# Kernel optimization log

Measured on AMD Instinct MI355X. Metric: run time of the kernel, lower is better.

The kernel has to match this reference:

```python
import jax, jax.numpy as jnp
import numpy as np

FEAT = 128
N_RBF = 20
CUTOFF = 5.0
NUM_CONV = 3
N_ATOMS = 8000
N_EDGES = 160000
N_MOLS = 100
EPS = 1e-15


def silu(x):
    return x * jax.nn.sigmoid(x)


def setup_inputs() -> dict:
    key = jax.random.key(0)
    ks = jax.random.split(key, 16)
    F = FEAT

    def w(k, shape, fan_in):
        return jax.random.normal(k, shape, dtype=jnp.float32) / np.sqrt(fan_in).astype(np.float32)

    nbr0 = jax.random.randint(ks[12], (N_EDGES,), 0, N_ATOMS)
    # avoid self-edges (would give zero distance)
    nbr1 = (nbr0 + 1 + jax.random.randint(ks[13], (N_EDGES,), 0, N_ATOMS - 1)) % N_ATOMS
    return {
        "xyz": jax.random.uniform(ks[0], (N_ATOMS, 3), dtype=jnp.float32) * 10.0,
        "emb_table": jax.random.normal(ks[1], (100, F), dtype=jnp.float32),
        "msg_w1": w(ks[2], (NUM_CONV, F, F), F),
        "msg_b1": jnp.zeros((NUM_CONV, F), jnp.float32),
        "msg_w2": w(ks[3], (NUM_CONV, F, 3 * F), F),
        "msg_b2": jnp.zeros((NUM_CONV, 3 * F), jnp.float32),
        "rbf_w": w(ks[4], (NUM_CONV, N_RBF, 3 * F), N_RBF),
        "rbf_b": jnp.zeros((NUM_CONV, 3 * F), jnp.float32),
        "upd_u": w(ks[5], (NUM_CONV, F, F), F),
        "upd_v": w(ks[6], (NUM_CONV, F, F), F),
        "upd_w1": w(ks[7], (NUM_CONV, 2 * F, F), 2 * F),
        "upd_b1": jnp.zeros((NUM_CONV, F), jnp.float32),
        "upd_w2": w(ks[8], (NUM_CONV, F, 3 * F), F),
        "upd_b2": jnp.zeros((NUM_CONV, 3 * F), jnp.float32),
        "ro_w1": w(ks[9], (F, F // 2), F),
        "ro_b1": jnp.zeros((F // 2,), jnp.float32),
        "ro_w2": w(ks[10], (F // 2, 1), F // 2),
        "ro_b2": jnp.zeros((1,), jnp.float32),
        "z": jax.random.randint(ks[11], (N_ATOMS,), 0, 100),
        "nbrs": jnp.stack([nbr0, nbr1], axis=1),
        "mol_idx": jnp.sort(jax.random.randint(ks[14], (N_ATOMS,), 0, N_MOLS)),
    }


def painn_forward(xyz, emb_table, msg_w1, msg_b1, msg_w2, msg_b2, rbf_w, rbf_b,
                  upd_u, upd_v, upd_w1, upd_b1, upd_w2, upd_b2,
                  ro_w1, ro_b1, ro_w2, ro_b2, z, nbrs, mol_idx):
    F = FEAT
    N = xyz.shape[0]
    # r_ij points from nbrs[:,0] (center i) to nbrs[:,1] (neighbor j)
    r_ij = xyz[nbrs[:, 1]] - xyz[nbrs[:, 0]]            # (E, 3)
    d = jnp.sqrt(jnp.sum(r_ij * r_ij, axis=-1))         # (E,)
    unit = r_ij / d[:, None]                            # (E, 3)
    # PaiNN sinc radial basis: sin(n*pi*d/cutoff)/d, n = 1..n_rbf
    n = jnp.arange(1, N_RBF + 1, dtype=jnp.float32)
    rbf = jnp.sin(n[None, :] * jnp.pi * d[:, None] / CUTOFF) / d[:, None]  # (E, n_rbf)
    # cosine cutoff envelope
    env = jnp.where(d <= CUTOFF, 0.5 * (jnp.cos(jnp.pi * d / CUTOFF) + 1.0), 0.0)

    s = emb_table[z]                                    # (N, F)
    v = jnp.zeros((N, F, 3), dtype=s.dtype)             # (N, F, 3)

    for i in range(NUM_CONV):
        # ---- message block ----
        phi = silu(s @ msg_w1[i] + msg_b1[i]) @ msg_w2[i] + msg_b2[i]   # (N, 3F)
        w_s = (rbf @ rbf_w[i] + rbf_b[i]) * env[:, None]                # (E, 3F)
        inv = (phi[nbrs[:, 1]] * w_s).reshape(-1, 3, F)                 # (E, 3, F)
        split0 = inv[:, 0, :][..., None]                                # (E, F, 1)
        split1 = inv[:, 1, :]                                           # (E, F)
        split2 = inv[:, 2, :][..., None]                                # (E, F, 1)
        dv_ij = split2 * unit[:, None, :] + split0 * v[nbrs[:, 1]]      # (E, F, 3)
        ds = jax.ops.segment_sum(split1, nbrs[:, 0], num_segments=N)
        dv = jax.ops.segment_sum(dv_ij, nbrs[:, 0], num_segments=N)
        s = s + ds
        v = v + dv
        # ---- update block ----
        u_v = jnp.einsum('nfd,fg->ngd', v, upd_u[i])                    # (N, F, 3)
        v_v = jnp.einsum('nfd,fg->ngd', v, upd_v[i])                    # (N, F, 3)
        v_v_norm = jnp.sqrt(jnp.sum(v_v * v_v, axis=-1) + EPS)          # (N, F)
        stack = jnp.concatenate([s, v_v_norm], axis=-1)                 # (N, 2F)
        a = (silu(stack @ upd_w1[i] + upd_b1[i]) @ upd_w2[i] + upd_b2[i]).reshape(-1, 3, F)
        a_vv = a[:, 0, :][..., None]
        a_sv = a[:, 1, :]
        a_ss = a[:, 2, :]
        dv_u = u_v * a_vv
        ds_u = jnp.sum(u_v * v_v, axis=-1) * a_sv + a_ss
        s = s + ds_u
        v = v + dv_u

    # readout MLP + per-molecule sum pool (SumPool)
    atom_e = silu(s @ ro_w1 + ro_b1) @ ro_w2 + ro_b2                    # (N, 1)
    energy = jax.ops.segment_sum(atom_e, mol_idx, num_segments=N_MOLS)  # (N_MOLS, 1)
    return energy


def reference(xyz, emb_table, msg_w1, msg_b1, msg_w2, msg_b2, rbf_w, rbf_b,
              upd_u, upd_v, upd_w1, upd_b1, upd_w2, upd_b2,
              ro_w1, ro_b1, ro_w2, ro_b2, z, nbrs, mol_idx):
    return painn_forward(xyz, emb_table, msg_w1, msg_b1, msg_w2, msg_b2, rbf_w, rbf_b,
                         upd_u, upd_v, upd_w1, upd_b1, upd_w2, upd_b2,
                         ro_w1, ro_b1, ro_w2, ro_b2, z, nbrs, mol_idx)
```

## Files before the change

### kernel.cpp

```cpp
#include <hip/hip_runtime.h>

static constexpr int F = 128;
static constexpr int N_RBF = 20;
static constexpr int N_ATOMS = 8000;
static constexpr int NP = 8064;
static constexpr int N_EDGES = 160000;
static constexpr int N_MOLS = 100;
static constexpr float CUTOFF = 5.0f;
static constexpr size_t NFC = (size_t)NP * F;
static constexpr int REC = 28;
#define PIF 3.14159265358979323846f

typedef __attribute__((ext_vector_type(8))) short bf16x8;
typedef __attribute__((ext_vector_type(4))) float f32x4;
typedef unsigned short ushort_t;
typedef unsigned int uint_t;

__device__ __forceinline__ float silu_f(float x) { return x / (1.f + __expf(-x)); }

__device__ __forceinline__ ushort_t f2bf(float x) {
    union { float f; uint_t u; } v; v.f = x;
    uint_t r = v.u + 0x7fffu + ((v.u >> 16) & 1u);
    return (ushort_t)(r >> 16);
}
__device__ __forceinline__ float bf2f(ushort_t h) {
    union { uint_t u; float f; } v; v.u = ((uint_t)h) << 16; return v.f;
}

__global__ __launch_bounds__(256) void count_kernel(
    const float* __restrict__ xyz, const int* __restrict__ nbrs,
    float* __restrict__ envb, int* __restrict__ cnt)
{
    int e = blockIdx.x * 256 + threadIdx.x;
    if (e >= N_EDGES) return;
    int i0 = nbrs[2*e+0], i1 = nbrs[2*e+1];
    float dx = xyz[3*i1+0] - xyz[3*i0+0];
    float dy = xyz[3*i1+1] - xyz[3*i0+1];
    float dz = xyz[3*i1+2] - xyz[3*i0+2];
    float d  = sqrtf(dx*dx + dy*dy + dz*dz);
    float ev = (d <= CUTOFF) ? 0.5f*(cosf(PIF*d/CUTOFF) + 1.f) : 0.f;
    envb[e] = ev;
    if (ev > 0.f) atomicAdd(&cnt[i0], 1);
}

__global__ __launch_bounds__(1024) void scan_kernel(
    const int* __restrict__ cnt, int* __restrict__ offsets, float* __restrict__ out)
{
    __shared__ int sums[1024];
    int tid = threadIdx.x;
    if (tid < N_MOLS) out[tid] = 0.f;
    int base = tid * 8;
    int local[8]; int s = 0;
    #pragma unroll
    for (int i = 0; i < 8; ++i) {
        int idx = base + i;
        local[i] = (idx < N_ATOMS) ? cnt[idx] : 0;
        s += local[i];
    }
    sums[tid] = s;
    __syncthreads();
    for (int d = 1; d < 1024; d <<= 1) {
        int v = (tid >= d) ? sums[tid - d] : 0;
        __syncthreads();
        sums[tid] += v;
        __syncthreads();
    }
    int ex = (tid == 0) ? 0 : sums[tid - 1];
    #pragma unroll
    for (int i = 0; i < 8; ++i) {
        int idx = base + i;
        if (idx < N_ATOMS) { offsets[idx] = ex; ex += local[i]; }
    }
}

__global__ __launch_bounds__(256) void build_kernel(
    const float* __restrict__ xyz, const int* __restrict__ nbrs,
    const float* __restrict__ envb, const int* __restrict__ offsets,
    int* __restrict__ cursor, float* __restrict__ rec)
{
    int e = blockIdx.x * 256 + threadIdx.x;
    if (e >= N_EDGES) return;
    float ev = envb[e];
    if (ev <= 0.f) return;
    int i0 = nbrs[2*e+0], i1 = nbrs[2*e+1];
    float dx = xyz[3*i1+0] - xyz[3*i0+0];
    float dy = xyz[3*i1+1] - xyz[3*i0+1];
    float dz = xyz[3*i1+2] - xyz[3*i0+2];
    float d  = sqrtf(dx*dx + dy*dy + dz*dz);
    float inv = 1.f / d;
    int pos = offsets[i0] + atomicAdd(&cursor[i0], 1);
    float* r = rec + (size_t)pos * REC;
    r[0] = __int_as_float(i1);
    r[1] = ev;
    r[2] = dx*inv; r[3] = dy*inv; r[4] = dz*inv;
    float base = PIF*d/CUTOFF;
    float sc = inv * ev;
    #pragma unroll
    for (int k = 0; k < N_RBF; ++k)
        r[5 + k] = sinf((float)(k+1)*base) * sc;
}

static constexpr int WPREP_W = 557056;
static constexpr int WPREP_TOTAL = 557184;
static constexpr int NATF = N_ATOMS * F;
static constexpr int PREP_TOTAL = NATF + WPREP_TOTAL + 2 * N_ATOMS;
__global__ __launch_bounds__(256) void prep_kernel(
    const float* __restrict__ emb, const int* __restrict__ z, float* __restrict__ s,
    const float* __restrict__ msg_w1, const float* __restrict__ msg_w2,
    const float* __restrict__ upd_u,  const float* __restrict__ upd_v,
    const float* __restrict__ upd_w1, const float* __restrict__ upd_w2,
    const float* __restrict__ ro_w1,  const float* __restrict__ ro_b1,
    ushort_t* __restrict__ dhi, ushort_t* __restrict__ dlo,
    float* __restrict__ robias, int* __restrict__ cntz)
{
    int gidx = blockIdx.x * 256 + threadIdx.x;
    if (gidx < NATF) {
        int n = gidx >> 7, f = gidx & 127;
        s[gidx] = emb[z[n]*F + f];
        return;
    }
    int idx = gidx - NATF;
    if (idx >= WPREP_TOTAL) {
        cntz[idx - WPREP_TOTAL] = 0;
        return;
    }
    if (idx >= WPREP_W) {
        int l = idx - WPREP_W;
        robias[l] = (l < 64) ? ro_b1[l] : 0.f;
        return;
    }
    float val;
    if (idx < 540672) {
        const float* src; int K, N, rem;
        if (idx < 49152)       { int l = idx;          int c = l / 16384; rem = l % 16384; K = 128; N = 128; src = msg_w1 + c * 16384; }
        else if (idx < 196608) { int l = idx - 49152;  int c = l / 49152; rem = l % 49152; K = 128; N = 384; src = msg_w2 + c * 49152; }
        else if (idx < 294912) { int l = idx - 196608; int c = l / 32768; rem = l % 32768; K = 128; N = 128;
                                 if (rem < 16384) src = upd_u + c * 16384;
                                 else { src = upd_v + c * 16384; rem -= 16384; } }
        else if (idx < 393216) { int l = idx - 294912; int c = l / 32768; rem = l % 32768; K = 256; N = 128; src = upd_w1 + c * 32768; }
        else                   { int l = idx - 393216; int c = l / 49152; rem = l % 49152; K = 128; N = 384; src = upd_w2 + c * 49152; }
        int n = rem / K, k = rem % K;
        val = src[k * N + n];
    } else {
        int l = idx - 540672;
        int n = l >> 7, k = l & 127;
        val = (n < 64) ? ro_w1[k * 64 + n] : 0.f;
    }
    ushort_t h = f2bf(val);
    dhi[idx] = h;
    dlo[idx] = f2bf(val - bf2f(h));
}

__global__ __launch_bounds__(256) void phi0_kernel(
    const float* __restrict__ sbuf,
    const ushort_t* __restrict__ W1h, const ushort_t* __restrict__ W1l,
    const float* __restrict__ b1,
    const ushort_t* __restrict__ W2h, const ushort_t* __restrict__ W2l,
    const float* __restrict__ b2,
    float* __restrict__ C)
{
    __shared__ __align__(16) ushort_t Ah[2][32 * 40], Al[2][32 * 40];
    __shared__ __align__(16) ushort_t Bh[2][128 * 40], Bl[2][128 * 40];
    __shared__ __align__(16) ushort_t Hh[32 * 136], Hl[32 * 136];
    const int tid = threadIdx.x;
    const int wave = tid >> 6, lane = tid & 63;
    const int row_l = lane & 15, quad = lane >> 4;
    const int wn = wave * 32;
    const int m0 = blockIdx.x * 32;
    const int lrA = tid >> 3, ksA = (tid & 7) * 4;
    const int lrB = tid >> 1, ksB = (tid & 1) * 16;

    float4 rx;
    uint4 b_h0, b_h1, b_l0, b_l1;

    auto loadB1 = [&](int k0) {
        const ushort_t* bh = &W1h[(size_t)lrB * 128 + k0 + ksB];
        const ushort_t* bl = &W1l[(size_t)lrB * 128 + k0 + ksB];
        b_h0 = *(const uint4*)bh; b_h1 = *(const uint4*)(bh + 8);
        b_l0 = *(const uint4*)bl; b_l1 = *(const uint4*)(bl + 8);
    };
    auto loadB2 = [&](int it2) {
        int ct = it2 >> 2, k0 = (it2 & 3) * 32;
        const ushort_t* bh = &W2h[(size_t)(ct * 128 + lrB) * 128 + k0 + ksB];
        const ushort_t* bl = &W2l[(size_t)(ct * 128 + lrB) * 128 + k0 + ksB];
        b_h0 = *(const uint4*)bh; b_h1 = *(const uint4*)(bh + 8);
        b_l0 = *(const uint4*)bl; b_l1 = *(const uint4*)(bl + 8);
    };
    auto writeA = [&](int buf) {
        float e[4] = {rx.x, rx.y, rx.z, rx.w};
        ushort_t ph[4], pl[4];
        #pragma unroll
        for (int t = 0; t < 4; ++t) {
            ushort_t h = f2bf(e[t]);
            ph[t] = h; pl[t] = f2bf(e[t] - bf2f(h));
        }
        *(uint2*)&Ah[buf][lrA * 40 + ksA] = *(uint2*)ph;
        *(uint2*)&Al[buf][lrA * 40 + ksA] = *(uint2*)pl;
    };
    auto writeB = [&](int buf) {
        *(uint4*)&Bh[buf][lrB * 40 + ksB]     = b_h0;
        *(uint4*)&Bh[buf][lrB * 40 + ksB + 8] = b_h1;
        *(uint4*)&Bl[buf][lrB * 40 + ksB]     = b_l0;
        *(uint4*)&Bl[buf][lrB * 40 + ksB + 8] = b_l1;
    };

    f32x4 acc[2][2];
    #pragma unroll
    for (int i = 0; i < 2; ++i)
        #pragma unroll
        for (int j = 0; j < 2; ++j)
            #pragma unroll
            for (int r = 0; r < 4; ++r) acc[i][j][r] = 0.f;

    rx = *(const float4*)&sbuf[(size_t)(m0 + lrA) * 128 + ksA];
    loadB1(0);
    writeA(0); writeB(0);
    __syncthreads();
    #pragma unroll
    for (int it = 0; it < 4; ++it) {
        const int k0n = (it + 1) * 32;
        if (it + 1 < 4) {
            rx = *(const float4*)&sbuf[(size_t)(m0 + lrA) * 128 + k0n + ksA];
            loadB1(k0n);
        }
        bf16x8 ahf[2], alf[2], bhf[2], blf[2];
        #pragma unroll
        for (int i = 0; i < 2; ++i) {
            int ar = (i * 16 + row_l) * 40 + quad * 8;
            ahf[i] = *(const bf16x8*)&Ah[it & 1][ar];
            alf[i] = *(const bf16x8*)&Al[it & 1][ar];
        }
        #pragma unroll
        for (int j = 0; j < 2; ++j) {
            int br = (wn + j * 16 + row_l) * 40 + quad * 8;
            bhf[j] = *(const bf16x8*)&Bh[it & 1][br];
            blf[j] = *(const bf16x8*)&Bl[it & 1][br];
        }
        #pragma unroll
        for (int i = 0; i < 2; ++i)
            #pragma unroll
            for (int j = 0; j < 2; ++j) {
                acc[i][j] = __builtin_amdgcn_mfma_f32_16x16x32_bf16(ahf[i], bhf[j], acc[i][j], 0, 0, 0);
                acc[i][j] = __builtin_amdgcn_mfma_f32_16x16x32_bf16(ahf[i], blf[j], acc[i][j], 0, 0, 0);
                acc[i][j] = __builtin_amdgcn_mfma_f32_16x16x32_bf16(alf[i], bhf[j], acc[i][j], 0, 0, 0);
            }
        if (it + 1 < 4) { writeA((it + 1) & 1); writeB((it + 1) & 1); }
        __syncthreads();
    }
    #pragma unroll
    for (int j = 0; j < 2; ++j) {
        int col = wn + j * 16 + row_l;
        float bval = b1[col];
        #pragma unroll
        for (int i = 0; i < 2; ++i)
            #pragma unroll
            for (int r = 0; r < 4; ++r) {
                int row = i * 16 + quad * 4 + r;
                float v = silu_f(acc[i][j][r] + bval);
                ushort_t h = f2bf(v);
                Hh[row * 136 + col] = h;
                Hl[row * 136 + col] = f2bf(v - bf2f(h));
            }
    }

    #pragma unroll
    for (int i = 0; i < 2; ++i)
        #pragma unroll
        for (int j = 0; j < 2; ++j)
            #pragma unroll
            for (int r = 0; r < 4; ++r) acc[i][j][r] = 0.f;
    loadB2(0); writeB(0);
    __syncthreads();
    #pragma unroll
    for (int it = 0; it < 12; ++it) {
        const int k0 = (it & 3) * 32;
        if (it + 1 < 12) loadB2(it + 1);
        bf16x8 ahf[2], alf[2], bhf[2], blf[2];
        #pragma unroll
        for (int i = 0; i < 2; ++i) {
            int ar = (i * 16 + row_l) * 136 + k0 + quad * 8;
            ahf[i] = *(const bf16x8*)&Hh[ar];
            alf[i] = *(const bf16x8*)&Hl[ar];
        }
        #pragma unroll
        for (int j = 0; j < 2; ++j) {
            int br = (wn + j * 16 + row_l) * 40 + quad * 8;
            bhf[j] = *(const bf16x8*)&Bh[it & 1][br];
            blf[j] = *(const bf16x8*)&Bl[it & 1][br];
        }
        #pragma unroll
        for (int i = 0; i < 2; ++i)
            #pragma unroll
            for (int j = 0; j < 2; ++j) {
                acc[i][j] = __builtin_amdgcn_mfma_f32_16x16x32_bf16(ahf[i], bhf[j], acc[i][j], 0, 0, 0);
                acc[i][j] = __builtin_amdgcn_mfma_f32_16x16x32_bf16(ahf[i], blf[j], acc[i][j], 0, 0, 0);
                acc[i][j] = __builtin_amdgcn_mfma_f32_16x16x32_bf16(alf[i], bhf[j], acc[i][j], 0, 0, 0);
            }
        if ((it & 3) == 3) {
            const int ct = it >> 2;
            #pragma unroll
            for (int j = 0; j < 2; ++j) {
                int col = ct * 128 + wn + j * 16 + row_l;
                float bval = b2[col];
                #pragma unroll
                for (int i = 0; i < 2; ++i)
                    #pragma unroll
                    for (int r = 0; r < 4; ++r) {
                        int row = i * 16 + quad * 4 + r;
                        C[(size_t)(m0 + row) * 384 + col] = acc[i][j][r] + bval;
                    }
            }
            #pragma unroll
            for (int i = 0; i < 2; ++i)
                #pragma unroll
                for (int j = 0; j < 2; ++j)
                    #pragma unroll
                    for (int r = 0; r < 4; ++r) acc[i][j][r] = 0.f;
        }
        if (it + 1 < 12) writeB((it + 1) & 1);
        __syncthreads();
    }
}

template<int TAIL>
__global__ __launch_bounds__(256) void updphi_kernel(
    float* __restrict__ s_io, float* __restrict__ v_io,
    const ushort_t* __restrict__ UVh, const ushort_t* __restrict__ UVl,
    const ushort_t* __restrict__ W1h, const ushort_t* __restrict__ W1l,
    const float* __restrict__ b1,
    const ushort_t* __restrict__ W2h, const ushort_t* __restrict__ W2l,
    const float* __restrict__ b2,
    const ushort_t* __restrict__ XW1h, const ushort_t* __restrict__ XW1l,
    const float* __restrict__ xb1,
    const ushort_t* __restrict__ XW2h, const ushort_t* __restrict__ XW2l,
    const float* __restrict__ xb2,
    float* __restrict__ phi_out,
    const float* __restrict__ w2ro, const float* __restrict__ b2ro,
    const int* __restrict__ mol, float* __restrict__ outp)
{
    __shared__ float uvv[96][260];
    __shared__ __align__(16) ushort_t Bh[2][128 * 40];
    __shared__ __align__(16) ushort_t Bl[2][128 * 40];
    __shared__ __align__(16) unsigned char AH[17408];
    __shared__ float molacc[128];
    __shared__ float redl[32][4];
    const int tid = threadIdx.x;
    const int wave = tid >> 6, lane = tid & 63;
    const int row_l = lane & 15, quad = lane >> 4;
    const int wn = wave * 32;
    const int m0 = blockIdx.x * 32;
    const int lrA = tid >> 3;
    const int ksA = (tid & 7) * 4;
    const int lrB = tid >> 1, ksB = (tid & 1) * 16;

    float* sS = &uvv[0][0];
    constexpr int SSTR = 132;

    {
        ushort_t* A0h = (ushort_t*)AH;
        ushort_t* A0l = A0h + 96 * 40;
        ushort_t* B0h = &Bh[0][0];
        ushort_t* B0l = &Bl[0][0];
        f32x4 acc0[6][4];
        #pragma unroll
        for (int i = 0; i < 6; ++i)
            #pragma unroll
            for (int j = 0; j < 4; ++j)
                #pragma unroll
                for (int r = 0; r < 4; ++r) acc0[i][j][r] = 0.f;
        for (int k0 = 0; k0 < 128; k0 += 32) {
            #pragma unroll
            for (int g = 0; g < 3; ++g) {
                int row = g * 32 + lrA;
                float4 v = *(const float4*)&v_io[(size_t)(m0 * 3 + row) * 128 + k0 + ksA];
                float e[4] = {v.x, v.y, v.z, v.w};
                ushort_t ph[4], pl[4];
                #pragma unroll
                for (int t = 0; t < 4; ++t) {
                    ushort_t h = f2bf(e[t]);
                    ph[t] = h; pl[t] = f2bf(e[t] - bf2f(h));
                }
                *(uint2*)&A0h[row * 40 + ksA] = *(uint2*)ph;
                *(uint2*)&A0l[row * 40 + ksA] = *(uint2*)pl;
            }
            {
                const ushort_t* bh = &UVh[(size_t)tid * 128 + k0];
                const ushort_t* bl = &UVl[(size_t)tid * 128 + k0];
                *(uint4*)&B0h[tid * 40 + 0]  = *(const uint4*)(bh + 0);
                *(uint4*)&B0h[tid * 40 + 8]  = *(const uint4*)(bh + 8);
                *(uint4*)&B0h[tid * 40 + 16] = *(const uint4*)(bh + 16);
                *(uint4*)&B0h[tid * 40 + 24] = *(const uint4*)(bh + 24);
                *(uint4*)&B0l[tid * 40 + 0]  = *(const uint4*)(bl + 0);
                *(uint4*)&B0l[tid * 40 + 8]  = *(const uint4*)(bl + 8);
                *(uint4*)&B0l[tid * 40 + 16] = *(const uint4*)(bl + 16);
                *(uint4*)&B0l[tid * 40 + 24] = *(const uint4*)(bl + 24);
            }
            __syncthreads();
            bf16x8 a0h[6], a0l[6], b0h[4], b0l[4];
            #pragma unroll
            for (int i = 0; i < 6; ++i) {
                int ar = (i * 16 + row_l) * 40 + quad * 8;
                a0h[i] = *(const bf16x8*)&A0h[ar];
                a0l[i] = *(const bf16x8*)&A0l[ar];
            }
            #pragma unroll
            for (int j = 0; j < 4; ++j) {
                int br = (wave * 64 + j * 16 + row_l) * 40 + quad * 8;
                b0h[j] = *(const bf16x8*)&B0h[br];
                b0l[j] = *(const bf16x8*)&B0l[br];
            }
            #pragma unroll
            for (int i = 0; i < 6; ++i)
                #pragma unroll
                for (int j = 0; j < 4; ++j) {
                    acc0[i][j] = __builtin_amdgcn_mfma_f32_16x16x32_bf16(a0h[i], b0h[j], acc0[i][j], 0, 0, 0);
                    acc0[i][j] = __builtin_amdgcn_mfma_f32_16x16x32_bf16(a0h[i], b0l[j], acc0[i][j], 0, 0, 0);
                    acc0[i][j] = __builtin_amdgcn_mfma_f32_16x16x32_bf16(a0l[i], b0h[j], acc0[i][j], 0, 0, 0);
                }
            __syncthreads();
        }
        #pragma unroll
        for (int i = 0; i < 6; ++i)
            #pragma unroll
            for (int j = 0; j < 4; ++j)
                #pragma unroll
                for (int r = 0; r < 4; ++r)
                    uvv[i * 16 + quad * 4 + r][wave * 64 + j * 16 + row_l] = acc0[i][j][r];
        __syncthreads();
    }

    ushort_t* Ah1 = (ushort_t*)AH;
    ushort_t* Al1 = Ah1 + 2 * 32 * 40;
    ushort_t* Hh  = (ushort_t*)AH;
    ushort_t* Hl  = Hh + 32 * 136;

    float4 rx;
    uint4 b_h0, b_h1, b_l0, b_l1;

    auto loadB1 = [&](int k0) {
        const ushort_t* bh = &W1h[(size_t)lrB * 256 + k0 + ksB];
        const ushort_t* bl = &W1l[(size_t)lrB * 256 + k0 + ksB];
        b_h0 = *(const uint4*)bh; b_h1 = *(const uint4*)(bh + 8);
        b_l0 = *(const uint4*)bl; b_l1 = *(const uint4*)(bl + 8);
    };
    auto writeB = [&](int buf) {
        *(uint4*)&Bh[buf][lrB * 40 + ksB]     = b_h0;
        *(uint4*)&Bh[buf][lrB * 40 + ksB + 8] = b_h1;
        *(uint4*)&Bl[buf][lrB * 40 + ksB]     = b_l0;
        *(uint4*)&Bl[buf][lrB * 40 + ksB + 8] = b_l1;
    };
    auto writeA1 = [&](int buf, int k0) {
        float e[4];
        if (k0 < 128) {
            e[0] = rx.x; e[1] = rx.y; e[2] = rx.z; e[3] = rx.w;
        } else {
            int f = k0 + ksA;
            #pragma unroll
            for (int t = 0; t < 4; ++t) {
                float x = uvv[lrA * 3 + 0][f + t];
                float y = uvv[lrA * 3 + 1][f + t];
                float z = uvv[lrA * 3 + 2][f + t];
                e[t] = sqrtf(x * x + y * y + z * z + 1e-15f);
            }
        }
        ushort_t ph[4], pl[4];
        #pragma unroll
        for (int t = 0; t < 4; ++t) {
            ushort_t h = f2bf(e[t]);
            ph[t] = h; pl[t] = f2bf(e[t] - bf2f(h));
        }
        *(uint2*)&Ah1[buf * 1280 + lrA * 40 + ksA] = *(uint2*)ph;
        *(uint2*)&Al1[buf * 1280 + lrA * 40 + ksA] = *(uint2*)pl;
    };

    f32x4 acc[2][2];
    #pragma unroll
    for (int i = 0; i < 2; ++i)
        #pragma unroll
        for (int j = 0; j < 2; ++j)
            #pragma unroll
            for (int r = 0; r < 4; ++r) acc[i][j][r] = 0.f;

    rx = *(const float4*)&s_io[(size_t)(m0 + lrA) * 128 + ksA];
    loadB1(0);
    writeA1(0, 0); writeB(0);
    __syncthreads();
    #pragma unroll
    for (int it = 0; it < 8; ++it) {
        const int k0n = (it + 1) * 32;
        if (it + 1 < 8) {
            if (k0n < 128) rx = *(const float4*)&s_io[(size_t)(m0 + lrA) * 128 + k0n + ksA];
            loadB1(k0n);
        }
        bf16x8 ahf[2], alf[2], bhf[2], blf[2];
        #pragma unroll
        for (int i = 0; i < 2; ++i) {
            int ar = (i * 16 + row_l) * 40 + quad * 8;
            ahf[i] = *(const bf16x8*)&Ah1[(it & 1) * 1280 + ar];
            alf[i] = *(const bf16x8*)&Al1[(it & 1) * 1280 + ar];
        }
        #pragma unroll
        for (int j = 0; j < 2; ++j) {
            int br = (wn + j * 16 + row_l) * 40 + quad * 8;
            bhf[j] = *(const bf16x8*)&Bh[it & 1][br];
            blf[j] = *(const bf16x8*)&Bl[it & 1][br];
        }
        #pragma unroll
        for (int i = 0; i < 2; ++i)
            #pragma unroll
            for (int j = 0; j < 2; ++j) {
                acc[i][j] = __builtin_amdgcn_mfma_f32_16x16x32_bf16(ahf[i], bhf[j], acc[i][j], 0, 0, 0);
                acc[i][j] = __builtin_amdgcn_mfma_f32_16x16x32_bf16(ahf[i], blf[j], acc[i][j], 0, 0, 0);
                acc[i][j] = __builtin_amdgcn_mfma_f32_16x16x32_bf16(alf[i], bhf[j], acc[i][j], 0, 0, 0);
            }
        if (it + 1 < 8) { writeA1((it + 1) & 1, k0n); writeB((it + 1) & 1); }
        __syncthreads();
    }
    #pragma unroll
    for (int j = 0; j < 2; ++j) {
        int col = wn + j * 16 + row_l;
        float bval = b1[col];
        #pragma unroll
        for (int i = 0; i < 2; ++i)
            #pragma unroll
            for (int r = 0; r < 4; ++r) {
                int row = i * 16 + quad * 4 + r;
                float v = silu_f(acc[i][j][r] + bval);
                ushort_t h = f2bf(v);
                Hh[row * 136 + col] = h;
                Hl[row * 136 + col] = f2bf(v - bf2f(h));
            }
    }

    constexpr int CT0 = TAIL ? 1 : 0;
    constexpr int NIT2 = (3 - CT0) * 4;
    auto loadB2 = [&](int it2) {
        int ct = CT0 + (it2 >> 2), k0 = (it2 & 3) * 32;
        const ushort_t* bh = &W2h[(size_t)(ct * 128 + lrB) * 128 + k0 + ksB];
        const ushort_t* bl = &W2l[(size_t)(ct * 128 + lrB) * 128 + k0 + ksB];
        b_h0 = *(const uint4*)bh; b_h1 = *(const uint4*)(bh + 8);
        b_l0 = *(const uint4*)bl; b_l1 = *(const uint4*)(bl + 8);
    };

    #pragma unroll
    for (int i = 0; i < 2; ++i)
        #pragma unroll
        for (int j = 0; j < 2; ++j)
            #pragma unroll
            for (int r = 0; r < 4; ++r) acc[i][j][r] = 0.f;
    f32x4 ssum[2][2];

    loadB2(0); writeB(0);
    __syncthreads();
    #pragma unroll
    for (int it = 0; it < NIT2; ++it) {
        const int k0 = (it & 3) * 32;
        if (it + 1 < NIT2) loadB2(it + 1);
        bf16x8 ahf[2], alf[2], bhf[2], blf[2];
        #pragma unroll
        for (int i = 0; i < 2; ++i) {
            int ar = (i * 16 + row_l) * 136 + k0 + quad * 8;
            ahf[i] = *(const bf16x8*)&Hh[ar];
            alf[i] = *(const bf16x8*)&Hl[ar];
        }
        #pragma unroll
        for (int j = 0; j < 2; ++j) {
            int br = (wn + j * 16 + row_l) * 40 + quad * 8;
            bhf[j] = *(const bf16x8*)&Bh[it & 1][br];
            blf[j] = *(const bf16x8*)&Bl[it & 1][br];
        }
        #pragma unroll
        for (int i = 0; i < 2; ++i)
            #pragma unroll
            for (int j = 0; j < 2; ++j) {
                acc[i][j] = __builtin_amdgcn_mfma_f32_16x16x32_bf16(ahf[i], bhf[j], acc[i][j], 0, 0, 0);
                acc[i][j] = __builtin_amdgcn_mfma_f32_16x16x32_bf16(ahf[i], blf[j], acc[i][j], 0, 0, 0);
                acc[i][j] = __builtin_amdgcn_mfma_f32_16x16x32_bf16(alf[i], bhf[j], acc[i][j], 0, 0, 0);
            }
        if ((it & 3) == 3) {
            const int ct = CT0 + (it >> 2);
            #pragma unroll
            for (int j = 0; j < 2; ++j) {
                int f = wn + j * 16 + row_l;
                float bval = b2[ct * 128 + f];
                #pragma unroll
                for (int i = 0; i < 2; ++i)
                    #pragma unroll
                    for (int r = 0; r < 4; ++r) {
                        int ln = i * 16 + quad * 4 + r;
                        float a = acc[i][j][r] + bval;
                        if (ct == 0) {
                            size_t vb = (size_t)(m0 + ln) * 3 * F + f;
                            v_io[vb]         += uvv[ln * 3 + 0][f] * a;
                            v_io[vb + F]     += uvv[ln * 3 + 1][f] * a;
                            v_io[vb + 2 * F] += uvv[ln * 3 + 2][f] * a;
                        } else if (ct == 1) {
                            float dot = uvv[ln * 3 + 0][f] * uvv[ln * 3 + 0][128 + f]
                                      + uvv[ln * 3 + 1][f] * uvv[ln * 3 + 1][128 + f]
                                      + uvv[ln * 3 + 2][f] * uvv[ln * 3 + 2][128 + f];
                            ssum[i][j][r] = dot * a;
                        } else {
                            float sv = s_io[(size_t)(m0 + ln) * F + f] + ssum[i][j][r] + a;
                            if constexpr (TAIL == 0) s_io[(size_t)(m0 + ln) * F + f] = sv;
                            sS[ln * SSTR + f] = sv;
                        }
                    }
            }
            #pragma unroll
            for (int i = 0; i < 2; ++i)
                #pragma unroll
                for (int j = 0; j < 2; ++j)
                    #pragma unroll
                    for (int r = 0; r < 4; ++r) acc[i][j][r] = 0.f;
        }
        if (it + 1 < NIT2) writeB((it + 1) & 1);
        __syncthreads();
    }

    if constexpr (TAIL == 1) { if (tid < 128) molacc[tid] = 0.f; }
    ushort_t* Ah3 = (ushort_t*)AH;
    ushort_t* Al3 = Ah3 + 2 * 1280;

    auto loadB31 = [&](int k0) {
        const ushort_t* bh = &XW1h[(size_t)lrB * 128 + k0 + ksB];
        const ushort_t* bl = &XW1l[(size_t)lrB * 128 + k0 + ksB];
        b_h0 = *(const uint4*)bh; b_h1 = *(const uint4*)(bh + 8);
        b_l0 = *(const uint4*)bl; b_l1 = *(const uint4*)(bl + 8);
    };
    auto writeA3 = [&](int buf, int k0) {
        float e[4];
        #pragma unroll
        for (int t = 0; t < 4; ++t) e[t] = sS[lrA * SSTR + k0 + ksA + t];
        ushort_t ph[4], pl[4];
        #pragma unroll
        for (int t = 0; t < 4; ++t) {
            ushort_t h = f2bf(e[t]);
            ph[t] = h; pl[t] = f2bf(e[t] - bf2f(h));
        }
        *(uint2*)&Ah3[buf * 1280 + lrA * 40 + ksA] = *(uint2*)ph;
        *(uint2*)&Al3[buf * 1280 + lrA * 40 + ksA] = *(uint2*)pl;
    };

    #pragma unroll
    for (int i = 0; i < 2; ++i)
        #pragma unroll
        for (int j = 0; j < 2; ++j)
            #pragma unroll
            for (int r = 0; r < 4; ++r) acc[i][j][r] = 0.f;

    loadB31(0);
    writeA3(0, 0); writeB(0);
    __syncthreads();
    #pragma unroll
    for (int it = 0; it < 4; ++it) {
        const int k0n = (it + 1) * 32;
        if (it + 1 < 4) loadB31(k0n);
        bf16x8 ahf[2], alf[2], bhf[2], blf[2];
        #pragma unroll
        for (int i = 0; i < 2; ++i) {
            int ar = (i * 16 + row_l) * 40 + quad * 8;
            ahf[i] = *(const bf16x8*)&Ah3[(it & 1) * 1280 + ar];
            alf[i] = *(const bf16x8*)&Al3[(it & 1) * 1280 + ar];
        }
        #pragma unroll
        for (int j = 0; j < 2; ++j) {
            int br = (wn + j * 16 + row_l) * 40 + quad * 8;
            bhf[j] = *(const bf16x8*)&Bh[it & 1][br];
            blf[j] = *(const bf16x8*)&Bl[it & 1][br];
        }
        #pragma unroll
        for (int i = 0; i < 2; ++i)
            #pragma unroll
            for (int j = 0; j < 2; ++j) {
                acc[i][j] = __builtin_amdgcn_mfma_f32_16x16x32_bf16(ahf[i], bhf[j], acc[i][j], 0, 0, 0);
                acc[i][j] = __builtin_amdgcn_mfma_f32_16x16x32_bf16(ahf[i], blf[j], acc[i][j], 0, 0, 0);
                acc[i][j] = __builtin_amdgcn_mfma_f32_16x16x32_bf16(alf[i], bhf[j], acc[i][j], 0, 0, 0);
            }
        if (it + 1 < 4) { writeA3((it + 1) & 1, k0n); writeB((it + 1) & 1); }
        __syncthreads();
    }

    if constexpr (TAIL == 0) {
        #pragma unroll
        for (int j = 0; j < 2; ++j) {
            int col = wn + j * 16 + row_l;
            float bval = xb1[col];
            #pragma unroll
            for (int i = 0; i < 2; ++i)
                #pragma unroll
                for (int r = 0; r < 4; ++r) {
                    int row = i * 16 + quad * 4 + r;
                    float v = silu_f(acc[i][j][r] + bval);
                    ushort_t h = f2bf(v);
                    Hh[row * 136 + col] = h;
                    Hl[row * 136 + col] = f2bf(v - bf2f(h));
                }
        }
        auto loadB32 = [&](int it2) {
            int ct = it2 >> 2, k0 = (it2 & 3) * 32;
            const ushort_t* bh = &XW2h[(size_t)(ct * 128 + lrB) * 128 + k0 + ksB];
            const ushort_t* bl = &XW2l[(size_t)(ct * 128 + lrB) * 128 + k0 + ksB];
            b_h0 = *(const uint4*)bh; b_h1 = *(const uint4*)(bh + 8);
            b_l0 = *(const uint4*)bl; b_l1 = *(const uint4*)(bl + 8);
        };
        #pragma unroll
        for (int i = 0; i < 2; ++i)
            #pragma unroll
            for (int j = 0; j < 2; ++j)
                #pragma unroll
                for (int r = 0; r < 4; ++r) acc[i][j][r] = 0.f;
        loadB32(0); writeB(0);
        __syncthreads();
        #pragma unroll
        for (int it = 0; it < 12; ++it) {
            const int k0 = (it & 3) * 32;
            if (it + 1 < 12) loadB32(it + 1);
            bf16x8 ahf[2], alf[2], bhf[2], blf[2];
            #pragma unroll
            for (int i = 0; i < 2; ++i) {
                int ar = (i * 16 + row_l) * 136 + k0 + quad * 8;
                ahf[i] = *(const bf16x8*)&Hh[ar];
                alf[i] = *(const bf16x8*)&Hl[ar];
            }
            #pragma unroll
            for (int j = 0; j < 2; ++j) {
                int br = (wn + j * 16 + row_l) * 40 + quad * 8;
                bhf[j] = *(const bf16x8*)&Bh[it & 1][br];
                blf[j] = *(const bf16x8*)&Bl[it & 1][br];
            }
            #pragma unroll
            for (int i = 0; i < 2; ++i)
                #pragma unroll
                for (int j = 0; j < 2; ++j) {
                    acc[i][j] = __builtin_amdgcn_mfma_f32_16x16x32_bf16(ahf[i], bhf[j], acc[i][j], 0, 0, 0);
                    acc[i][j] = __builtin_amdgcn_mfma_f32_16x16x32_bf16(ahf[i], blf[j], acc[i][j], 0, 0, 0);
                    acc[i][j] = __builtin_amdgcn_mfma_f32_16x16x32_bf16(alf[i], bhf[j], acc[i][j], 0, 0, 0);
                }
            if ((it & 3) == 3) {
                const int ct = it >> 2;
                #pragma unroll
                for (int j = 0; j < 2; ++j) {
                    int col = ct * 128 + wn + j * 16 + row_l;
                    float bval = xb2[col];
                    #pragma unroll
                    for (int i = 0; i < 2; ++i)
                        #pragma unroll
                        for (int r = 0; r < 4; ++r) {
                            int row = i * 16 + quad * 4 + r;
                            phi_out[(size_t)(m0 + row) * 384 + col] = acc[i][j][r] + bval;
                        }
                }
                #pragma unroll
                for (int i = 0; i < 2; ++i)
                    #pragma unroll
                    for (int j = 0; j < 2; ++j)
                        #pragma unroll
                        for (int r = 0; r < 4; ++r) acc[i][j][r] = 0.f;
            }
            if (it + 1 < 12) writeB((it + 1) & 1);
            __syncthreads();
        }
    } else {
        float part[2][4];
        #pragma unroll
        for (int i = 0; i < 2; ++i)
            #pragma unroll
            for (int r = 0; r < 4; ++r) part[i][r] = 0.f;
        #pragma unroll
        for (int j = 0; j < 2; ++j) {
            int col = wn + j * 16 + row_l;
            float bv = xb1[col];
            float wv = (col < 64) ? w2ro[col] : 0.f;
            #pragma unroll
            for (int i = 0; i < 2; ++i)
                #pragma unroll
                for (int r = 0; r < 4; ++r)
                    part[i][r] += silu_f(acc[i][j][r] + bv) * wv;
        }
        #pragma unroll
        for (int o = 1; o < 16; o <<= 1)
            #pragma unroll
            for (int i = 0; i < 2; ++i)
                #pragma unroll
                for (int r = 0; r < 4; ++r)
                    part[i][r] += __shfl_xor(part[i][r], o);
        if (row_l == 0)
            #pragma unroll
            for (int i = 0; i < 2; ++i)
                #pragma unroll
                for (int r = 0; r < 4; ++r)
                    redl[i * 16 + quad * 4 + r][wave] = part[i][r];
        __syncthreads();
        if (tid < 32) {
            int n = m0 + tid;
            if (n < N_ATOMS) {
                float e = redl[tid][0] + redl[tid][1] + redl[tid][2] + redl[tid][3] + b2ro[0];
                atomicAdd(&molacc[mol[n]], e);
            }
        }
        __syncthreads();
        if (tid < 100 && molacc[tid] != 0.f) atomicAdd(&outp[tid], molacc[tid]);
    }
}

template<int ZVIN>
__global__ __launch_bounds__(128) void msg_gather(
    const float* __restrict__ phi, const float* __restrict__ rec,
    const float* __restrict__ rbf_w, const float* __restrict__ rbf_b,
    const float* __restrict__ v_in, float* __restrict__ s,
    float* __restrict__ v_out, const int* __restrict__ offsets,
    const int* __restrict__ cnt)
{
    const int n = blockIdx.x, tid = threadIdx.x;
    float W0[N_RBF], W1[N_RBF], W2[N_RBF];
    #pragma unroll
    for (int k = 0; k < N_RBF; ++k) {
        W0[k] = rbf_w[k*3*F + tid];
        W1[k] = rbf_w[k*3*F + F + tid];
        W2[k] = rbf_w[k*3*F + 2*F + tid];
    }
    const float b0 = rbf_b[tid], b1 = rbf_b[F + tid], b2 = rbf_b[2*F + tid];
    float ds = 0.f, dvx = 0.f, dvy = 0.f, dvz = 0.f;
    const int off = offsets[n], c = cnt[n];
    const float* r = rec + (size_t)off * REC;
    #pragma unroll 2
    for (int t = 0; t < c; ++t, r += REC) {
        int j = __float_as_int(r[0]);
        float ev = r[1];
        float ux = r[2], uy = r[3], uz = r[4];
        float w0 = b0 * ev, w1 = b1 * ev, w2 = b2 * ev;
        #pragma unroll
        for (int k = 0; k < N_RBF; ++k) {
            float rk = r[5 + k];
            w0 += rk * W0[k]; w1 += rk * W1[k]; w2 += rk * W2[k];
        }
        const float* prow = phi + (size_t)j * 3 * F;
        float s0 = prow[tid] * w0;
        float s1 = prow[F + tid] * w1;
        float s2 = prow[2*F + tid] * w2;
        ds  += s1;
        if constexpr (ZVIN) {
            dvx += s2*ux; dvy += s2*uy; dvz += s2*uz;
        } else {
            const float* vrow = v_in + (size_t)j * 3 * F;
            dvx += s2*ux + s0 * vrow[tid];
            dvy += s2*uy + s0 * vrow[F + tid];
            dvz += s2*uz + s0 * vrow[2*F + tid];
        }
    }
    s[(size_t)n * F + tid] += ds;
    size_t vb = (size_t)n * 3 * F + tid;
    if constexpr (ZVIN) {
        v_out[vb]       = dvx;
        v_out[vb + F]   = dvy;
        v_out[vb + 2*F] = dvz;
    } else {
        v_out[vb]       = v_in[vb]       + dvx;
        v_out[vb + F]   = v_in[vb + F]   + dvy;
        v_out[vb + 2*F] = v_in[vb + 2*F] + dvz;
    }
}

extern "C" void kernel_launch(void* const* d_in, const int* in_sizes, int n_in,
                              void* d_out, int out_size, void* d_ws, size_t ws_size,
                              hipStream_t stream)
{
    const float* xyz    = (const float*)d_in[0];
    const float* emb    = (const float*)d_in[1];
    const float* msg_w1 = (const float*)d_in[2];
    const float* msg_b1 = (const float*)d_in[3];
    const float* msg_w2 = (const float*)d_in[4];
    const float* msg_b2 = (const float*)d_in[5];
    const float* rbf_w  = (const float*)d_in[6];
    const float* rbf_b  = (const float*)d_in[7];
    const float* upd_u  = (const float*)d_in[8];
    const float* upd_v  = (const float*)d_in[9];
    const float* upd_w1 = (const float*)d_in[10];
    const float* upd_b1 = (const float*)d_in[11];
    const float* upd_w2 = (const float*)d_in[12];
    const float* upd_b2 = (const float*)d_in[13];
    const float* ro_w1  = (const float*)d_in[14];
    const float* ro_b1  = (const float*)d_in[15];
    const float* ro_w2  = (const float*)d_in[16];
    const float* ro_b2  = (const float*)d_in[17];
    const int*   z      = (const int*)d_in[18];
    const int*   nbrs   = (const int*)d_in[19];
    const int*   molidx = (const int*)d_in[20];
    float* out = (float*)d_out;

    float* ws = (float*)d_ws;
    size_t off = 0;
    auto alloc = [&](size_t n) { float* p = ws + off; off += n; return p; };
    float* s_buf   = alloc(NFC);
    float* v1_buf  = alloc(3 * NFC);
    float* v2_buf  = alloc(3 * NFC);
    float* phi_buf = alloc(3 * NFC);
    float* envb    = alloc(N_EDGES);
    float* edgerec = alloc((size_t)N_EDGES * REC);
    ushort_t* wbf_hi = (ushort_t*)alloc(WPREP_W / 2 + 64);
    ushort_t* wbf_lo = (ushort_t*)alloc(WPREP_W / 2 + 64);
    float* robias   = alloc(128);
    int* cnt        = (int*)alloc(N_ATOMS);
    int* cursor     = (int*)alloc(N_ATOMS);
    int* offsets    = (int*)alloc(N_ATOMS);

    const size_t oW1 = 0, oW2 = 49152, oUV = 196608, oU1 = 294912, oU2 = 393216, oRO = 540672;

    prep_kernel<<<dim3(PREP_TOTAL / 256), dim3(256), 0, stream>>>(
        emb, z, s_buf,
        msg_w1, msg_w2, upd_u, upd_v, upd_w1, upd_w2, ro_w1, ro_b1,
        wbf_hi, wbf_lo, robias, cnt);
    count_kernel<<<dim3((N_EDGES + 255) / 256), dim3(256), 0, stream>>>(
        xyz, nbrs, envb, cnt);
    scan_kernel<<<dim3(1), dim3(1024), 0, stream>>>(cnt, offsets, out);
    build_kernel<<<dim3((N_EDGES + 255) / 256), dim3(256), 0, stream>>>(
        xyz, nbrs, envb, offsets, cursor, edgerec);

    phi0_kernel<<<dim3(NP/32), dim3(256), 0, stream>>>(
        s_buf,
        wbf_hi + oW1, wbf_lo + oW1, msg_b1,
        wbf_hi + oW2, wbf_lo + oW2, msg_b2,
        phi_buf);

    float* vin = v1_buf;
    float* vout = v2_buf;
    for (int i = 0; i < 3; ++i) {
        if (i == 0)
            msg_gather<1><<<dim3(N_ATOMS), dim3(128), 0, stream>>>(
                phi_buf, edgerec, rbf_w + (size_t)i*N_RBF*3*F, rbf_b + (size_t)i*3*F,
                vin, s_buf, vout, offsets, cnt);
        else
            msg_gather<0><<<dim3(N_ATOMS), dim3(128), 0, stream>>>(
                phi_buf, edgerec, rbf_w + (size_t)i*N_RBF*3*F, rbf_b + (size_t)i*3*F,
                vin, s_buf, vout, offsets, cnt);
        if (i < 2) {
            updphi_kernel<0><<<dim3(NP/32), dim3(256), 0, stream>>>(
                s_buf, vout,
                wbf_hi + oUV + (size_t)i*32768, wbf_lo + oUV + (size_t)i*32768,
                wbf_hi + oU1 + (size_t)i*32768, wbf_lo + oU1 + (size_t)i*32768,
                upd_b1 + (size_t)i*F,
                wbf_hi + oU2 + (size_t)i*49152, wbf_lo + oU2 + (size_t)i*49152,
                upd_b2 + (size_t)i*3*F,
                wbf_hi + oW1 + (size_t)(i+1)*16384, wbf_lo + oW1 + (size_t)(i+1)*16384,
                msg_b1 + (size_t)(i+1)*F,
                wbf_hi + oW2 + (size_t)(i+1)*49152, wbf_lo + oW2 + (size_t)(i+1)*49152,
                msg_b2 + (size_t)(i+1)*3*F,
                phi_buf,
                nullptr, nullptr, nullptr, nullptr);
        } else {
            updphi_kernel<1><<<dim3(NP/32), dim3(256), 0, stream>>>(
                s_buf, vout,
                wbf_hi + oUV + (size_t)i*32768, wbf_lo + oUV + (size_t)i*32768,
                wbf_hi + oU1 + (size_t)i*32768, wbf_lo + oU1 + (size_t)i*32768,
                upd_b1 + (size_t)i*F,
                wbf_hi + oU2 + (size_t)i*49152, wbf_lo + oU2 + (size_t)i*49152,
                upd_b2 + (size_t)i*3*F,
                wbf_hi + oRO, wbf_lo + oRO, robias,
                nullptr, nullptr, nullptr,
                nullptr,
                ro_w2, ro_b2, molidx, out);
        }
        float* tmp = vin; vin = vout; vout = tmp;
    }
}
```

Measured before the change: 327.8 us.

## Fuse message gather into update/phi kernel per 32-atom tile

Merges the per-atom message gather kernel into the update+phi GEMM kernel. Each 256-thread block processes the edges of its 32 atoms, accumulates ds and dv into shared memory with LDS atomics, and feeds the updated v straight into the U/V GEMM without a round trip through global memory. Phi is double-buffered (phiA/phiB) because neighbours read the previous phi while other blocks write the new one. This cuts three kernel launches and the v write/read traffic, but per-block edge work becomes uneven, LDS atomics add contention, and the larger fused kernel may lower occupancy.

New measurement: 660.2 us. 2.01x slower.

```diff
diff --git a/kernel.cpp b/kernel.cpp
--- a/kernel.cpp
+++ b/kernel.cpp
@@ -71,6 +71,7 @@
         int idx = base + i;
         if (idx < N_ATOMS) { offsets[idx] = ex; ex += local[i]; }
     }
+    if (tid == 1023) offsets[N_ATOMS] = ex;
 }
 
 __global__ __launch_bounds__(256) void build_kernel(
@@ -98,6 +99,7 @@
     #pragma unroll
     for (int k = 0; k < N_RBF; ++k)
         r[5 + k] = sinf((float)(k+1)*base) * sc;
+    r[25] = __int_as_float(i0);
 }
 
 static constexpr int WPREP_W = 557056;
@@ -322,9 +324,12 @@
     }
 }
 
-template<int TAIL>
-__global__ __launch_bounds__(256) void updphi_kernel(
-    float* __restrict__ s_io, float* __restrict__ v_io,
+template<int ZVIN, int TAIL>
+__global__ __launch_bounds__(256) void conv_kernel(
+    float* __restrict__ s_io, const float* __restrict__ vin, float* __restrict__ vout,
+    const float* __restrict__ phin, const float* __restrict__ rec,
+    const int* __restrict__ offsets,
+    const float* __restrict__ rbf_w, const float* __restrict__ rbf_b,
     const ushort_t* __restrict__ UVh, const ushort_t* __restrict__ UVl,
     const ushort_t* __restrict__ W1h, const ushort_t* __restrict__ W1l,
     const float* __restrict__ b1,
@@ -338,7 +343,7 @@
     const float* __restrict__ w2ro, const float* __restrict__ b2ro,
     const int* __restrict__ mol, float* __restrict__ outp)
 {
-    __shared__ float uvv[96][260];
+    __shared__ __align__(16) float uvv[96][260];
     __shared__ __align__(16) ushort_t Bh[2][128 * 40];
     __shared__ __align__(16) ushort_t Bl[2][128 * 40];
     __shared__ __align__(16) unsigned char AH[17408];
@@ -356,6 +361,90 @@
     float* sS = &uvv[0][0];
     constexpr int SSTR = 132;
 
+    uint4 b_h0, b_h1, b_l0, b_l1;
+    auto writeB = [&](int buf) {
+        *(uint4*)&Bh[buf][lrB * 40 + ksB]     = b_h0;
+        *(uint4*)&Bh[buf][lrB * 40 + ksB + 8] = b_h1;
+        *(uint4*)&Bl[buf][lrB * 40 + ksB]     = b_l0;
+        *(uint4*)&Bl[buf][lrB * 40 + ksB + 8] = b_l1;
+    };
+
+    {
+        float4 z4; z4.x = 0.f; z4.y = 0.f; z4.z = 0.f; z4.w = 0.f;
+        for (int t = tid; t < 96 * 32; t += 256) {
+            int row = t >> 5, c4 = (t & 31) * 4;
+            *(float4*)&uvv[row][c4] = z4;
+        }
+        for (int t = tid; t < 32 * 32; t += 256) {
+            int ln = t >> 5, c4 = (t & 31) * 4;
+            *(float4*)&uvv[ln][128 + c4] = z4;
+        }
+        __syncthreads();
+        if (m0 < N_ATOMS) {
+            const int eBeg = offsets[m0];
+            const int eEnd = offsets[(m0 + 32 < N_ATOMS) ? (m0 + 32) : N_ATOMS];
+            const int g = tid >> 7;
+            const int f = tid & 127;
+            float Wk0[N_RBF], Wk1[N_RBF], Wk2[N_RBF];
+            #pragma unroll
+            for (int k = 0; k < N_RBF; ++k) {
+                Wk0[k] = rbf_w[k * 384 + f];
+                Wk1[k] = rbf_w[k * 384 + 128 + f];
+                Wk2[k] = rbf_w[k * 384 + 256 + f];
+            }
+            const float bb0 = rbf_b[f], bb1 = rbf_b[128 + f], bb2 = rbf_b[256 + f];
+            #pragma unroll 4
+            for (int e = eBeg + g; e < eEnd; e += 2) {
+                const float* r = rec + (size_t)e * REC;
+                const int jj = __float_as_int(r[0]);
+                const float ev = r[1];
+                const float ux = r[2], uy = r[3], uz = r[4];
+                const int ln = __float_as_int(r[25]) - m0;
+                float w0 = bb0 * ev, w1 = bb1 * ev, w2 = bb2 * ev;
+                #pragma unroll
+                for (int k = 0; k < N_RBF; ++k) {
+                    const float rk = r[5 + k];
+                    w0 += rk * Wk0[k]; w1 += rk * Wk1[k]; w2 += rk * Wk2[k];
+                }
+                const float* prow = phin + (size_t)jj * 384;
+                const float s0 = prow[f] * w0;
+                const float s1 = prow[128 + f] * w1;
+                const float s2 = prow[256 + f] * w2;
+                float dx = s2 * ux, dy = s2 * uy, dz = s2 * uz;
+                if constexpr (!ZVIN) {
+                    const float* vr = vin + (size_t)jj * 384;
+                    dx += s0 * vr[f];
+                    dy += s0 * vr[128 + f];
+                    dz += s0 * vr[256 + f];
+                }
+                atomicAdd(&uvv[ln][128 + f], s1);
+                atomicAdd(&uvv[ln * 3 + 0][f], dx);
+                atomicAdd(&uvv[ln * 3 + 1][f], dy);
+                atomicAdd(&uvv[ln * 3 + 2][f], dz);
+            }
+        }
+        __syncthreads();
+        for (int t = tid; t < 96 * 32; t += 256) {
+            int row = t >> 5, c4 = (t & 31) * 4;
+            float4 av = *(float4*)&uvv[row][c4];
+            if constexpr (!ZVIN) {
+                float4 pv = *(const float4*)&vin[(size_t)(m0 * 3 + row) * 128 + c4];
+                av.x += pv.x; av.y += pv.y; av.z += pv.z; av.w += pv.w;
+                *(float4*)&uvv[row][c4] = av;
+            }
+            if constexpr (TAIL == 0)
+                *(float4*)&vout[(size_t)(m0 * 3 + row) * 128 + c4] = av;
+        }
+        for (int t = tid; t < 32 * 32; t += 256) {
+            int ln = t >> 5, c4 = (t & 31) * 4;
+            float4 as = *(float4*)&uvv[ln][128 + c4];
+            float4 sv = *(const float4*)&s_io[(size_t)(m0 + ln) * 128 + c4];
+            sv.x += as.x; sv.y += as.y; sv.z += as.z; sv.w += as.w;
+            *(float4*)&s_io[(size_t)(m0 + ln) * 128 + c4] = sv;
+        }
+        __syncthreads();
+    }
+
     {
         ushort_t* A0h = (ushort_t*)AH;
         ushort_t* A0l = A0h + 96 * 40;
@@ -363,16 +452,16 @@
         ushort_t* B0l = &Bl[0][0];
         f32x4 acc0[6][4];
         #pragma unroll
-        for (int i = 0; i < 6; ++i)
+        for (int i2 = 0; i2 < 6; ++i2)
             #pragma unroll
             for (int j = 0; j < 4; ++j)
                 #pragma unroll
-                for (int r = 0; r < 4; ++r) acc0[i][j][r] = 0.f;
+                for (int r = 0; r < 4; ++r) acc0[i2][j][r] = 0.f;
         for (int k0 = 0; k0 < 128; k0 += 32) {
             #pragma unroll
-            for (int g = 0; g < 3; ++g) {
-                int row = g * 32 + lrA;
-                float4 v = *(const float4*)&v_io[(size_t)(m0 * 3 + row) * 128 + k0 + ksA];
+            for (int g2 = 0; g2 < 3; ++g2) {
+                int row = g2 * 32 + lrA;
+                float4 v = *(const float4*)&uvv[row][k0 + ksA];
                 float e[4] = {v.x, v.y, v.z, v.w};
                 ushort_t ph[4], pl[4];
                 #pragma unroll
@@ -398,10 +487,10 @@
             __syncthreads();
             bf16x8 a0h[6], a0l[6], b0h[4], b0l[4];
             #pragma unroll
-            for (int i = 0; i < 6; ++i) {
-                int ar = (i * 16 + row_l) * 40 + quad * 8;
-                a0h[i] = *(const bf16x8*)&A0h[ar];
-                a0l[i] = *(const bf16x8*)&A0l[ar];
+            for (int i2 = 0; i2 < 6; ++i2) {
+                int ar = (i2 * 16 + row_l) * 40 + quad * 8;
+                a0h[i2] = *(const bf16x8*)&A0h[ar];
+                a0l[i2] = *(const bf16x8*)&A0l[ar];
             }
             #pragma unroll
             for (int j = 0; j < 4; ++j) {
@@ -410,211 +499,203 @@
                 b0l[j] = *(const bf16x8*)&B0l[br];
             }
             #pragma unroll
-            for (int i = 0; i < 6; ++i)
+            for (int i2 = 0; i2 < 6; ++i2)
                 #pragma unroll
                 for (int j = 0; j < 4; ++j) {
-                    acc0[i][j] = __builtin_amdgcn_mfma_f32_16x16x32_bf16(a0h[i], b0h[j], acc0[i][j], 0, 0, 0);
-                    acc0[i][j] = __builtin_amdgcn_mfma_f32_16x16x32_bf16(a0h[i], b0l[j], acc0[i][j], 0, 0, 0);
-                    acc0[i][j] = __builtin_amdgcn_mfma_f32_16x16x32_bf16(a0l[i], b0h[j], acc0[i][j], 0, 0, 0);
+                    acc0[i2][j] = __builtin_amdgcn_mfma_f32_16x16x32_bf16(a0h[i2], b0h[j], acc0[i2][j], 0, 0, 0);
+                    acc0[i2][j] = __builtin_amdgcn_mfma_f32_16x16x32_bf16(a0h[i2], b0l[j], acc0[i2][j], 0, 0, 0);
+                    acc0[i2][j] = __builtin_amdgcn_mfma_f32_16x16x32_bf16(a0l[i2], b0h[j], acc0[i2][j], 0, 0, 0);
                 }
             __syncthreads();
         }
         #pragma unroll
-        for (int i = 0; i < 6; ++i)
+        for (int i2 = 0; i2 < 6; ++i2)
             #pragma unroll
             for (int j = 0; j < 4; ++j)
                 #pragma unroll
                 for (int r = 0; r < 4; ++r)
-                    uvv[i * 16 + quad * 4 + r][wave * 64 + j * 16 + row_l] = acc0[i][j][r];
-        __syncthreads();
-    }
-
-    ushort_t* Ah1 = (ushort_t*)AH;
-    ushort_t* Al1 = Ah1 + 2 * 32 * 40;
-    ushort_t* Hh  = (ushort_t*)AH;
-    ushort_t* Hl  = Hh + 32 * 136;
-
-    float4 rx;
-    uint4 b_h0, b_h1, b_l0, b_l1;
-
-    auto loadB1 = [&](int k0) {
-        const ushort_t* bh = &W1h[(size_t)lrB * 256 + k0 + ksB];
-        const ushort_t* bl = &W1l[(size_t)lrB * 256 + k0 + ksB];
-        b_h0 = *(const uint4*)bh; b_h1 = *(const uint4*)(bh + 8);
-        b_l0 = *(const uint4*)bl; b_l1 = *(const uint4*)(bl + 8);
-    };
-    auto writeB = [&](int buf) {
-        *(uint4*)&Bh[buf][lrB * 40 + ksB]     = b_h0;
-        *(uint4*)&Bh[buf][lrB * 40 + ksB + 8] = b_h1;
-        *(uint4*)&Bl[buf][lrB * 40 + ksB]     = b_l0;
-        *(uint4*)&Bl[buf][lrB * 40 + ksB + 8] = b_l1;
-    };
-    auto writeA1 = [&](int buf, int k0) {
-        float e[4];
-        if (k0 < 128) {
-            e[0] = rx.x; e[1] = rx.y; e[2] = rx.z; e[3] = rx.w;
-        } else {
-            int f = k0 + ksA;
+                    uvv[i2 * 16 + quad * 4 + r][wave * 64 + j * 16 + row_l] = acc0[i2][j][r];
+        __syncthreads();
+    }
+
+    ushort_t* Hh = (ushort_t*)AH;
+    ushort_t* Hl = Hh + 32 * 136;
+    {
+        ushort_t* Ah1 = (ushort_t*)AH;
+        ushort_t* Al1 = Ah1 + 2 * 1280;
+        float4 rx;
+        auto loadB1u = [&](int k0) {
+            const ushort_t* bh = &W1h[(size_t)lrB * 256 + k0 + ksB];
+            const ushort_t* bl = &W1l[(size_t)lrB * 256 + k0 + ksB];
+            b_h0 = *(const uint4*)bh; b_h1 = *(const uint4*)(bh + 8);
+            b_l0 = *(const uint4*)bl; b_l1 = *(const uint4*)(bl + 8);
+        };
+        auto writeA1 = [&](int buf, int k0) {
+            float e[4];
+            if (k0 < 128) {
+                e[0] = rx.x; e[1] = rx.y; e[2] = rx.z; e[3] = rx.w;
+            } else {
+                int fo = k0 + ksA;
+                #pragma unroll
+                for (int t = 0; t < 4; ++t) {
+                    float x = uvv[lrA * 3 + 0][fo + t];
+                    float y = uvv[lrA * 3 + 1][fo + t];
+                    float z = uvv[lrA * 3 + 2][fo + t];
+                    e[t] = sqrtf(x * x + y * y + z * z + 1e-15f);
+                }
+            }
+            ushort_t ph[4], pl[4];
             #pragma unroll
             for (int t = 0; t < 4; ++t) {
-                float x = uvv[lrA * 3 + 0][f + t];
-                float y = uvv[lrA * 3 + 1][f + t];
-                float z = uvv[lrA * 3 + 2][f + t];
-                e[t] = sqrtf(x * x + y * y + z * z + 1e-15f);
-            }
-        }
-        ushort_t ph[4], pl[4];
-        #pragma unroll
-        for (int t = 0; t < 4; ++t) {
-            ushort_t h = f2bf(e[t]);
-            ph[t] = h; pl[t] = f2bf(e[t] - bf2f(h));
-        }
-        *(uint2*)&Ah1[buf * 1280 + lrA * 40 + ksA] = *(uint2*)ph;
-        *(uint2*)&Al1[buf * 1280 + lrA * 40 + ksA] = *(uint2*)pl;
-    };
-
-    f32x4 acc[2][2];
-    #pragma unroll
-    for (int i = 0; i < 2; ++i)
-        #pragma unroll
-        for (int j = 0; j < 2; ++j)
-            #pragma unroll
-            for (int r = 0; r < 4; ++r) acc[i][j][r] = 0.f;
-
-    rx = *(const float4*)&s_io[(size_t)(m0 + lrA) * 128 + ksA];
-    loadB1(0);
-    writeA1(0, 0); writeB(0);
-    __syncthreads();
-    #pragma unroll
-    for (int it = 0; it < 8; ++it) {
-        const int k0n = (it + 1) * 32;
-        if (it + 1 < 8) {
-            if (k0n < 128) rx = *(const float4*)&s_io[(size_t)(m0 + lrA) * 128 + k0n + ksA];
-            loadB1(k0n);
-        }
-        bf16x8 ahf[2], alf[2], bhf[2], blf[2];
-        #pragma unroll
-        for (int i = 0; i < 2; ++i) {
-            int ar = (i * 16 + row_l) * 40 + quad * 8;
-            ahf[i] = *(const bf16x8*)&Ah1[(it & 1) * 1280 + ar];
-            alf[i] = *(const bf16x8*)&Al1[(it & 1) * 1280 + ar];
+                ushort_t h = f2bf(e[t]);
+                ph[t] = h; pl[t] = f2bf(e[t] - bf2f(h));
+            }
+            *(uint2*)&Ah1[buf * 1280 + lrA * 40 + ksA] = *(uint2*)ph;
+            *(uint2*)&Al1[buf * 1280 + lrA * 40 + ksA] = *(uint2*)pl;
+        };
+        f32x4 acc[2][2];
+        #pragma unroll
+        for (int i2 = 0; i2 < 2; ++i2)
+            #pragma unroll
+            for (int j = 0; j < 2; ++j)
+                #pragma unroll
+                for (int r = 0; r < 4; ++r) acc[i2][j][r] = 0.f;
+        rx = *(const float4*)&s_io[(size_t)(m0 + lrA) * 128 + ksA];
+        loadB1u(0);
+        writeA1(0, 0); writeB(0);
+        __syncthreads();
+        #pragma unroll
+        for (int it = 0; it < 8; ++it) {
+            const int k0n = (it + 1) * 32;
+            if (it + 1 < 8) {
+                if (k0n < 128) rx = *(const float4*)&s_io[(size_t)(m0 + lrA) * 128 + k0n + ksA];
+                loadB1u(k0n);
+            }
+            bf16x8 ahf[2], alf[2], bhf[2], blf[2];
+            #pragma unroll
+            for (int i2 = 0; i2 < 2; ++i2) {
+                int ar = (it & 1) * 1280 + (i2 * 16 + row_l) * 40 + quad * 8;
+                ahf[i2] = *(const bf16x8*)&Ah1[ar];
+                alf[i2] = *(const bf16x8*)&Al1[ar];
+            }
+            #pragma unroll
+            for (int j = 0; j < 2; ++j) {
+                int br = (wn + j * 16 + row_l) * 40 + quad * 8;
+                bhf[j] = *(const bf16x8*)&Bh[it & 1][br];
+                blf[j] = *(const bf16x8*)&Bl[it & 1][br];
+            }
+            #pragma unroll
+            for (int i2 = 0; i2 < 2; ++i2)
+                #pragma unroll
+                for (int j = 0; j < 2; ++j) {
+                    acc[i2][j] = __builtin_amdgcn_mfma_f32_16x16x32_bf16(ahf[i2], bhf[j], acc[i2][j], 0, 0, 0);
+                    acc[i2][j] = __builtin_amdgcn_mfma_f32_16x16x32_bf16(ahf[i2], blf[j], acc[i2][j], 0, 0, 0);
+                    acc[i2][j] = __builtin_amdgcn_mfma_f32_16x16x32_bf16(alf[i2], bhf[j], acc[i2][j], 0, 0, 0);
+                }
+            if (it + 1 < 8) { writeA1((it + 1) & 1, k0n); writeB((it + 1) & 1); }
+            __syncthreads();
         }
         #pragma unroll
         for (int j = 0; j < 2; ++j) {
-            int br = (wn + j * 16 + row_l) * 40 + quad * 8;
-            bhf[j] = *(const bf16x8*)&Bh[it & 1][br];
-            blf[j] = *(const bf16x8*)&Bl[it & 1][br];
-        }
-        #pragma unroll
-        for (int i = 0; i < 2; ++i)
-            #pragma unroll
-            for (int j = 0; j < 2; ++j) {
-                acc[i][j] = __builtin_amdgcn_mfma_f32_16x16x32_bf16(ahf[i], bhf[j], acc[i][j], 0, 0, 0);
-                acc[i][j] = __builtin_amdgcn_mfma_f32_16x16x32_bf16(ahf[i], blf[j], acc[i][j], 0, 0, 0);
-                acc[i][j] = __builtin_amdgcn_mfma_f32_16x16x32_bf16(alf[i], bhf[j], acc[i][j], 0, 0, 0);
-            }
-        if (it + 1 < 8) { writeA1((it + 1) & 1, k0n); writeB((it + 1) & 1); }
-        __syncthreads();
-    }
-    #pragma unroll
-    for (int j = 0; j < 2; ++j) {
-        int col = wn + j * 16 + row_l;
-        float bval = b1[col];
-        #pragma unroll
-        for (int i = 0; i < 2; ++i)
-            #pragma unroll
-            for (int r = 0; r < 4; ++r) {
-                int row = i * 16 + quad * 4 + r;
-                float v = silu_f(acc[i][j][r] + bval);
-                ushort_t h = f2bf(v);
-                Hh[row * 136 + col] = h;
-                Hl[row * 136 + col] = f2bf(v - bf2f(h));
-            }
+            int col = wn + j * 16 + row_l;
+            float bval = b1[col];
+            #pragma unroll
+            for (int i2 = 0; i2 < 2; ++i2)
+                #pragma unroll
+                for (int r = 0; r < 4; ++r) {
+                    int row = i2 * 16 + quad * 4 + r;
+                    float v = silu_f(acc[i2][j][r] + bval);
+                    ushort_t h = f2bf(v);
+                    Hh[row * 136 + col] = h;
+                    Hl[row * 136 + col] = f2bf(v - bf2f(h));
+                }
+        }
     }
 
     constexpr int CT0 = TAIL ? 1 : 0;
     constexpr int NIT2 = (3 - CT0) * 4;
-    auto loadB2 = [&](int it2) {
-        int ct = CT0 + (it2 >> 2), k0 = (it2 & 3) * 32;
-        const ushort_t* bh = &W2h[(size_t)(ct * 128 + lrB) * 128 + k0 + ksB];
-        const ushort_t* bl = &W2l[(size_t)(ct * 128 + lrB) * 128 + k0 + ksB];
-        b_h0 = *(const uint4*)bh; b_h1 = *(const uint4*)(bh + 8);
-        b_l0 = *(const uint4*)bl; b_l1 = *(const uint4*)(bl + 8);
-    };
-
-    #pragma unroll
-    for (int i = 0; i < 2; ++i)
-        #pragma unroll
-        for (int j = 0; j < 2; ++j)
-            #pragma unroll
-            for (int r = 0; r < 4; ++r) acc[i][j][r] = 0.f;
-    f32x4 ssum[2][2];
-
-    loadB2(0); writeB(0);
-    __syncthreads();
-    #pragma unroll
-    for (int it = 0; it < NIT2; ++it) {
-        const int k0 = (it & 3) * 32;
-        if (it + 1 < NIT2) loadB2(it + 1);
-        bf16x8 ahf[2], alf[2], bhf[2], blf[2];
-        #pragma unroll
-        for (int i = 0; i < 2; ++i) {
-            int ar = (i * 16 + row_l) * 136 + k0 + quad * 8;
-            ahf[i] = *(const bf16x8*)&Hh[ar];
-            alf[i] = *(const bf16x8*)&Hl[ar];
-        }
-        #pragma unroll
-        for (int j = 0; j < 2; ++j) {
-            int br = (wn + j * 16 + row_l) * 40 + quad * 8;
-            bhf[j] = *(const bf16x8*)&Bh[it & 1][br];
-            blf[j] = *(const bf16x8*)&Bl[it & 1][br];
-        }
-        #pragma unroll
-        for (int i = 0; i < 2; ++i)
+    {
+        auto loadB2u = [&](int it2) {
+            int ct = CT0 + (it2 >> 2), k0 = (it2 & 3) * 32;
+            const ushort_t* bh = &W2h[(size_t)(ct * 128 + lrB) * 128 + k0 + ksB];
+            const ushort_t* bl = &W2l[(size_t)(ct * 128 + lrB) * 128 + k0 + ksB];
+            b_h0 = *(const uint4*)bh; b_h1 = *(const uint4*)(bh + 8);
+            b_l0 = *(const uint4*)bl; b_l1 = *(const uint4*)(bl + 8);
+        };
+        f32x4 acc[2][2];
+        #pragma unroll
+        for (int i2 = 0; i2 < 2; ++i2)
+            #pragma unroll
+            for (int j = 0; j < 2; ++j)
+                #pragma unroll
+                for (int r = 0; r < 4; ++r) acc[i2][j][r] = 0.f;
+        f32x4 ssum[2][2];
+        loadB2u(0); writeB(0);
+        __syncthreads();
+        #pragma unroll
+        for (int it = 0; it < NIT2; ++it) {
+            const int k0 = (it & 3) * 32;
+            if (it + 1 < NIT2) loadB2u(it + 1);
+            bf16x8 ahf[2], alf[2], bhf[2], blf[2];
+            #pragma unroll
+            for (int i2 = 0; i2 < 2; ++i2) {
+                int ar = (i2 * 16 + row_l) * 136 + k0 + quad * 8;
+                ahf[i2] = *(const bf16x8*)&Hh[ar];
+                alf[i2] = *(const bf16x8*)&Hl[ar];
+            }
             #pragma unroll
             for (int j = 0; j < 2; ++j) {
-                acc[i][j] = __builtin_amdgcn_mfma_f32_16x16x32_bf16(ahf[i], bhf[j], acc[i][j], 0, 0, 0);
-                acc[i][j] = __builtin_amdgcn_mfma_f32_16x16x32_bf16(ahf[i], blf[j], acc[i][j], 0, 0, 0);
-                acc[i][j] = __builtin_amdgcn_mfma_f32_16x16x32_bf16(alf[i], bhf[j], acc[i][j], 0, 0, 0);
-            }
-        if ((it & 3) == 3) {
-            const int ct = CT0 + (it >> 2);
-            #pragma unroll
-            for (int j = 0; j < 2; ++j) {
-                int f = wn + j * 16 + row_l;
-                float bval = b2[ct * 128 + f];
-                #pragma unroll
-                for (int i = 0; i < 2; ++i)
+                int br = (wn + j * 16 + row_l) * 40 + quad * 8;
+                bhf[j] = *(const bf16x8*)&Bh[it & 1][br];
+                blf[j] = *(const bf16x8*)&Bl[it & 1][br];
+            }
+            #pragma unroll
+            for (int i2 = 0; i2 < 2; ++i2)
+                #pragma unroll
+                for (int j = 0; j < 2; ++j) {
+                    acc[i2][j] = __builtin_amdgcn_mfma_f32_16x16x32_bf16(ahf[i2], bhf[j], acc[i2][j], 0, 0, 0);
+                    acc[i2][j] = __builtin_amdgcn_mfma_f32_16x16x32_bf16(ahf[i2], blf[j], acc[i2][j], 0, 0, 0);
+                    acc[i2][j] = __builtin_amdgcn_mfma_f32_16x16x32_bf16(alf[i2], bhf[j], acc[i2][j], 0, 0, 0);
+                }
+            if ((it & 3) == 3) {
+                const int ct = CT0 + (it >> 2);
+                #pragma unroll
+                for (int j = 0; j < 2; ++j) {
+                    int f_ = wn + j * 16 + row_l;
+                    float bval = b2[ct * 128 + f_];
                     #pragma unroll
-                    for (int r = 0; r < 4; ++r) {
-                        int ln = i * 16 + quad * 4 + r;
-                        float a = acc[i][j][r] + bval;
-                        if (ct == 0) {
-                            size_t vb = (size_t)(m0 + ln) * 3 * F + f;
-                            v_io[vb]         += uvv[ln * 3 + 0][f] * a;
-                            v_io[vb + F]     += uvv[ln * 3 + 1][f] * a;
-                            v_io[vb + 2 * F] += uvv[ln * 3 + 2][f] * a;
-                        } else if (ct == 1) {
-                            float dot = uvv[ln * 3 + 0][f] * uvv[ln * 3 + 0][128 + f]
-                                      + uvv[ln * 3 + 1][f] * uvv[ln * 3 + 1][128 + f]
-                                      + uvv[ln * 3 + 2][f] * uvv[ln * 3 + 2][128 + f];
-                            ssum[i][j][r] = dot * a;
-                        } else {
-                            float sv = s_io[(size_t)(m0 + ln) * F + f] + ssum[i][j][r] + a;
-                            if constexpr (TAIL == 0) s_io[(size_t)(m0 + ln) * F + f] = sv;
-                            sS[ln * SSTR + f] = sv;
+                    for (int i2 = 0; i2 < 2; ++i2)
+                        #pragma unroll
+                        for (int r = 0; r < 4; ++r) {
+                            int ln = i2 * 16 + quad * 4 + r;
+                            float a = acc[i2][j][r] + bval;
+                            if (ct == 0) {
+                                size_t vb = (size_t)(m0 + ln) * 384 + f_;
+                                vout[vb]       += uvv[ln*3+0][f_] * a;
+                                vout[vb + 128] += uvv[ln*3+1][f_] * a;
+                                vout[vb + 256] += uvv[ln*3+2][f_] * a;
+                            } else if (ct == 1) {
+                                float dot = uvv[ln*3+0][f_] * uvv[ln*3+0][128+f_]
+                                          + uvv[ln*3+1][f_] * uvv[ln*3+1][128+f_]
+                                          + uvv[ln*3+2][f_] * uvv[ln*3+2][128+f_];
+                                ssum[i2][j][r] = dot * a;
+                            } else {
+                                float sv = s_io[(size_t)(m0+ln)*128 + f_] + ssum[i2][j][r] + a;
+                                if constexpr (TAIL == 0) s_io[(size_t)(m0+ln)*128 + f_] = sv;
+                                sS[ln * SSTR + f_] = sv;
+                            }
                         }
-                    }
-            }
-            #pragma unroll
-            for (int i = 0; i < 2; ++i)
-                #pragma unroll
-                for (int j = 0; j < 2; ++j)
+                }
+                #pragma unroll
+                for (int i2 = 0; i2 < 2; ++i2)
                     #pragma unroll
-                    for (int r = 0; r < 4; ++r) acc[i][j][r] = 0.f;
-        }
-        if (it + 1 < NIT2) writeB((it + 1) & 1);
-        __syncthreads();
+                    for (int j = 0; j < 2; ++j)
+                        #pragma unroll
+                        for (int r = 0; r < 4; ++r) acc[i2][j][r] = 0.f;
+            }
+            if (it + 1 < NIT2) writeB((it + 1) & 1);
+            __syncthreads();
+        }
     }
 
     if constexpr (TAIL == 1) { if (tid < 128) molacc[tid] = 0.f; }
@@ -641,12 +722,13 @@
         *(uint2*)&Al3[buf * 1280 + lrA * 40 + ksA] = *(uint2*)pl;
     };
 
+    f32x4 acc[2][2];
     #pragma unroll
-    for (int i = 0; i < 2; ++i)
+    for (int i2 = 0; i2 < 2; ++i2)
         #pragma unroll
         for (int j = 0; j < 2; ++j)
             #pragma unroll
-            for (int r = 0; r < 4; ++r) acc[i][j][r] = 0.f;
+            for (int r = 0; r < 4; ++r) acc[i2][j][r] = 0.f;
 
     loadB31(0);
     writeA3(0, 0); writeB(0);
@@ -657,10 +739,10 @@
         if (it + 1 < 4) loadB31(k0n);
         bf16x8 ahf[2], alf[2], bhf[2], blf[2];
         #pragma unroll
-        for (int i = 0; i < 2; ++i) {
-            int ar = (i * 16 + row_l) * 40 + quad * 8;
-            ahf[i] = *(const bf16x8*)&Ah3[(it & 1) * 1280 + ar];
-            alf[i] = *(const bf16x8*)&Al3[(it & 1) * 1280 + ar];
+        for (int i2 = 0; i2 < 2; ++i2) {
+            int ar = (it & 1) * 1280 + (i2 * 16 + row_l) * 40 + quad * 8;
+            ahf[i2] = *(const bf16x8*)&Ah3[ar];
+            alf[i2] = *(const bf16x8*)&Al3[ar];
         }
         #pragma unroll
         for (int j = 0; j < 2; ++j) {
@@ -669,12 +751,12 @@
             blf[j] = *(const bf16x8*)&Bl[it & 1][br];
         }
         #pragma unroll
-        for (int i = 0; i < 2; ++i)
+        for (int i2 = 0; i2 < 2; ++i2)
             #pragma unroll
             for (int j = 0; j < 2; ++j) {
-                acc[i][j] = __builtin_amdgcn_mfma_f32_16x16x32_bf16(ahf[i], bhf[j], acc[i][j], 0, 0, 0);
-                acc[i][j] = __builtin_amdgcn_mfma_f32_16x16x32_bf16(ahf[i], blf[j], acc[i][j], 0, 0, 0);
-                acc[i][j] = __builtin_amdgcn_mfma_f32_16x16x32_bf16(alf[i], bhf[j], acc[i][j], 0, 0, 0);
+                acc[i2][j] = __builtin_amdgcn_mfma_f32_16x16x32_bf16(ahf[i2], bhf[j], acc[i2][j], 0, 0, 0);
+                acc[i2][j] = __builtin_amdgcn_mfma_f32_16x16x32_bf16(ahf[i2], blf[j], acc[i2][j], 0, 0, 0);
+                acc[i2][j] = __builtin_amdgcn_mfma_f32_16x16x32_bf16(alf[i2], bhf[j], acc[i2][j], 0, 0, 0);
             }
         if (it + 1 < 4) { writeA3((it + 1) & 1, k0n); writeB((it + 1) & 1); }
         __syncthreads();
@@ -686,11 +768,11 @@
             int col = wn + j * 16 + row_l;
             float bval = xb1[col];
             #pragma unroll
-            for (int i = 0; i < 2; ++i)
+            for (int i2 = 0; i2 < 2; ++i2)
                 #pragma unroll
                 for (int r = 0; r < 4; ++r) {
-                    int row = i * 16 + quad * 4 + r;
-                    float v = silu_f(acc[i][j][r] + bval);
+                    int row = i2 * 16 + quad * 4 + r;
+                    float v = silu_f(acc[i2][j][r] + bval);
                     ushort_t h = f2bf(v);
                     Hh[row * 136 + col] = h;
                     Hl[row * 136 + col] = f2bf(v - bf2f(h));
@@ -704,11 +786,11 @@
             b_l0 = *(const uint4*)bl; b_l1 = *(const uint4*)(bl + 8);
         };
         #pragma unroll
-        for (int i = 0; i < 2; ++i)
+        for (int i2 = 0; i2 < 2; ++i2)
             #pragma unroll
             for (int j = 0; j < 2; ++j)
                 #pragma unroll
-                for (int r = 0; r < 4; ++r) acc[i][j][r] = 0.f;
+                for (int r = 0; r < 4; ++r) acc[i2][j][r] = 0.f;
         loadB32(0); writeB(0);
         __syncthreads();
         #pragma unroll
@@ -717,10 +799,10 @@
             if (it + 1 < 12) loadB32(it + 1);
             bf16x8 ahf[2], alf[2], bhf[2], blf[2];
             #pragma unroll
-            for (int i = 0; i < 2; ++i) {
-                int ar = (i * 16 + row_l) * 136 + k0 + quad * 8;
-                ahf[i] = *(const bf16x8*)&Hh[ar];
-                alf[i] = *(const bf16x8*)&Hl[ar];
+            for (int i2 = 0; i2 < 2; ++i2) {
+                int ar = (i2 * 16 + row_l) * 136 + k0 + quad * 8;
+                ahf[i2] = *(const bf16x8*)&Hh[ar];
+                alf[i2] = *(const bf16x8*)&Hl[ar];
             }
             #pragma unroll
             for (int j = 0; j < 2; ++j) {
@@ -729,12 +811,12 @@
                 blf[j] = *(const bf16x8*)&Bl[it & 1][br];
             }
             #pragma unroll
-            for (int i = 0; i < 2; ++i)
+            for (int i2 = 0; i2 < 2; ++i2)
                 #pragma unroll
                 for (int j = 0; j < 2; ++j) {
-                    acc[i][j] = __builtin_amdgcn_mfma_f32_16x16x32_bf16(ahf[i], bhf[j], acc[i][j], 0, 0, 0);
-                    acc[i][j] = __builtin_amdgcn_mfma_f32_16x16x32_bf16(ahf[i], blf[j], acc[i][j], 0, 0, 0);
-                    acc[i][j] = __builtin_amdgcn_mfma_f32_16x16x32_bf16(alf[i], bhf[j], acc[i][j], 0, 0, 0);
+                    acc[i2][j] = __builtin_amdgcn_mfma_f32_16x16x32_bf16(ahf[i2], bhf[j], acc[i2][j], 0, 0, 0);
+                    acc[i2][j] = __builtin_amdgcn_mfma_f32_16x16x32_bf16(ahf[i2], blf[j], acc[i2][j], 0, 0, 0);
+                    acc[i2][j] = __builtin_amdgcn_mfma_f32_16x16x32_bf16(alf[i2], bhf[j], acc[i2][j], 0, 0, 0);
                 }
             if ((it & 3) == 3) {
                 const int ct = it >> 2;
@@ -743,19 +825,19 @@
                     int col = ct * 128 + wn + j * 16 + row_l;
                     float bval = xb2[col];
                     #pragma unroll
-                    for (int i = 0; i < 2; ++i)
+                    for (int i2 = 0; i2 < 2; ++i2)
                         #pragma unroll
                         for (int r = 0; r < 4; ++r) {
-                            int row = i * 16 + quad * 4 + r;
-                            phi_out[(size_t)(m0 + row) * 384 + col] = acc[i][j][r] + bval;
+                            int row = i2 * 16 + quad * 4 + r;
+                            phi_out[(size_t)(m0 + row) * 384 + col] = acc[i2][j][r] + bval;
                         }
                 }
                 #pragma unroll
-                for (int i = 0; i < 2; ++i)
+                for (int i2 = 0; i2 < 2; ++i2)
                     #pragma unroll
                     for (int j = 0; j < 2; ++j)
                         #pragma unroll
-                        for (int r = 0; r < 4; ++r) acc[i][j][r] = 0.f;
+                        for (int r = 0; r < 4; ++r) acc[i2][j][r] = 0.f;
             }
             if (it + 1 < 12) writeB((it + 1) & 1);
             __syncthreads();
@@ -763,101 +845,43 @@
     } else {
         float part[2][4];
         #pragma unroll
-        for (int i = 0; i < 2; ++i)
-            #pragma unroll
-            for (int r = 0; r < 4; ++r) part[i][r] = 0.f;
+        for (int i2 = 0; i2 < 2; ++i2)
+            #pragma unroll
+            for (int r = 0; r < 4; ++r) part[i2][r] = 0.f;
         #pragma unroll
         for (int j = 0; j < 2; ++j) {
             int col = wn + j * 16 + row_l;
             float bv = xb1[col];
             float wv = (col < 64) ? w2ro[col] : 0.f;
             #pragma unroll
-            for (int i = 0; i < 2; ++i)
+            for (int i2 = 0; i2 < 2; ++i2)
                 #pragma unroll
                 for (int r = 0; r < 4; ++r)
-                    part[i][r] += silu_f(acc[i][j][r] + bv) * wv;
+                    part[i2][r] += silu_f(acc[i2][j][r] + bv) * wv;
         }
         #pragma unroll
         for (int o = 1; o < 16; o <<= 1)
             #pragma unroll
-            for (int i = 0; i < 2; ++i)
+            for (int i2 = 0; i2 < 2; ++i2)
                 #pragma unroll
                 for (int r = 0; r < 4; ++r)
-                    part[i][r] += __shfl_xor(part[i][r], o);
+                    part[i2][r] += __shfl_xor(part[i2][r], o);
         if (row_l == 0)
             #pragma unroll
-            for (int i = 0; i < 2; ++i)
+            for (int i2 = 0; i2 < 2; ++i2)
                 #pragma unroll
                 for (int r = 0; r < 4; ++r)
-                    redl[i * 16 + quad * 4 + r][wave] = part[i][r];
+                    redl[i2 * 16 + quad * 4 + r][wave] = part[i2][r];
         __syncthreads();
         if (tid < 32) {
             int n = m0 + tid;
             if (n < N_ATOMS) {
-                float e = redl[tid][0] + redl[tid][1] + redl[tid][2] + redl[tid][3] + b2ro[0];
-                atomicAdd(&molacc[mol[n]], e);
+                float ee = redl[tid][0] + redl[tid][1] + redl[tid][2] + redl[tid][3] + b2ro[0];
+                atomicAdd(&molacc[mol[n]], ee);
             }
         }
         __syncthreads();
         if (tid < 100 && molacc[tid] != 0.f) atomicAdd(&outp[tid], molacc[tid]);
-    }
-}
-
-template<int ZVIN>
-__global__ __launch_bounds__(128) void msg_gather(
-    const float* __restrict__ phi, const float* __restrict__ rec,
-    const float* __restrict__ rbf_w, const float* __restrict__ rbf_b,
-    const float* __restrict__ v_in, float* __restrict__ s,
-    float* __restrict__ v_out, const int* __restrict__ offsets,
-    const int* __restrict__ cnt)
-{
-    const int n = blockIdx.x, tid = threadIdx.x;
-    float W0[N_RBF], W1[N_RBF], W2[N_RBF];
-    #pragma unroll
-    for (int k = 0; k < N_RBF; ++k) {
-        W0[k] = rbf_w[k*3*F + tid];
-        W1[k] = rbf_w[k*3*F + F + tid];
-        W2[k] = rbf_w[k*3*F + 2*F + tid];
-    }
-    const float b0 = rbf_b[tid], b1 = rbf_b[F + tid], b2 = rbf_b[2*F + tid];
-    float ds = 0.f, dvx = 0.f, dvy = 0.f, dvz = 0.f;
-    const int off = offsets[n], c = cnt[n];
-    const float* r = rec + (size_t)off * REC;
-    #pragma unroll 2
-    for (int t = 0; t < c; ++t, r += REC) {
-        int j = __float_as_int(r[0]);
-        float ev = r[1];
-        float ux = r[2], uy = r[3], uz = r[4];
-        float w0 = b0 * ev, w1 = b1 * ev, w2 = b2 * ev;
-        #pragma unroll
-        for (int k = 0; k < N_RBF; ++k) {
-            float rk = r[5 + k];
-            w0 += rk * W0[k]; w1 += rk * W1[k]; w2 += rk * W2[k];
-        }
-        const float* prow = phi + (size_t)j * 3 * F;
-        float s0 = prow[tid] * w0;
-        float s1 = prow[F + tid] * w1;
-        float s2 = prow[2*F + tid] * w2;
-        ds  += s1;
-        if constexpr (ZVIN) {
-            dvx += s2*ux; dvy += s2*uy; dvz += s2*uz;
-        } else {
-            const float* vrow = v_in + (size_t)j * 3 * F;
-            dvx += s2*ux + s0 * vrow[tid];
-            dvy += s2*uy + s0 * vrow[F + tid];
-            dvz += s2*uz + s0 * vrow[2*F + tid];
-        }
-    }
-    s[(size_t)n * F + tid] += ds;
-    size_t vb = (size_t)n * 3 * F + tid;
-    if constexpr (ZVIN) {
-        v_out[vb]       = dvx;
-        v_out[vb + F]   = dvy;
-        v_out[vb + 2*F] = dvz;
-    } else {
-        v_out[vb]       = v_in[vb]       + dvx;
-        v_out[vb + F]   = v_in[vb + F]   + dvy;
-        v_out[vb + 2*F] = v_in[vb + 2*F] + dvz;
     }
 }
 
@@ -892,9 +916,10 @@
     size_t off = 0;
     auto alloc = [&](size_t n) { float* p = ws + off; off += n; return p; };
     float* s_buf   = alloc(NFC);
+    float* v0_buf  = alloc(3 * NFC);
     float* v1_buf  = alloc(3 * NFC);
-    float* v2_buf  = alloc(3 * NFC);
-    float* phi_buf = alloc(3 * NFC);
+    float* phiA    = alloc(3 * NFC);
+    float* phiB    = alloc(3 * NFC);
     float* envb    = alloc(N_EDGES);
     float* edgerec = alloc((size_t)N_EDGES * REC);
     ushort_t* wbf_hi = (ushort_t*)alloc(WPREP_W / 2 + 64);
@@ -902,11 +927,11 @@
     float* robias   = alloc(128);
     int* cnt        = (int*)alloc(N_ATOMS);
     int* cursor     = (int*)alloc(N_ATOMS);
-    int* offsets    = (int*)alloc(N_ATOMS);
+    int* offsets    = (int*)alloc(N_ATOMS + 1);
 
     const size_t oW1 = 0, oW2 = 49152, oUV = 196608, oU1 = 294912, oU2 = 393216, oRO = 540672;
 
-    prep_kernel<<<dim3(PREP_TOTAL / 256), dim3(256), 0, stream>>>(
+    prep_kernel<<<dim3((PREP_TOTAL + 255) / 256), dim3(256), 0, stream>>>(
         emb, z, s_buf,
         msg_w1, msg_w2, upd_u, upd_v, upd_w1, upd_w2, ro_w1, ro_b1,
         wbf_hi, wbf_lo, robias, cnt);
@@ -920,46 +945,41 @@
         s_buf,
         wbf_hi + oW1, wbf_lo + oW1, msg_b1,
         wbf_hi + oW2, wbf_lo + oW2, msg_b2,
-        phi_buf);
-
-    float* vin = v1_buf;
-    float* vout = v2_buf;
-    for (int i = 0; i < 3; ++i) {
-        if (i == 0)
-            msg_gather<1><<<dim3(N_ATOMS), dim3(128), 0, stream>>>(
-                phi_buf, edgerec, rbf_w + (size_t)i*N_RBF*3*F, rbf_b + (size_t)i*3*F,
-                vin, s_buf, vout, offsets, cnt);
-        else
-            msg_gather<0><<<dim3(N_ATOMS), dim3(128), 0, stream>>>(
-                phi_buf, edgerec, rbf_w + (size_t)i*N_RBF*3*F, rbf_b + (size_t)i*3*F,
-                vin, s_buf, vout, offsets, cnt);
-        if (i < 2) {
-            updphi_kernel<0><<<dim3(NP/32), dim3(256), 0, stream>>>(
-                s_buf, vout,
-                wbf_hi + oUV + (size_t)i*32768, wbf_lo + oUV + (size_t)i*32768,
-                wbf_hi + oU1 + (size_t)i*32768, wbf_lo + oU1 + (size_t)i*32768,
-                upd_b1 + (size_t)i*F,
-                wbf_hi + oU2 + (size_t)i*49152, wbf_lo + oU2 + (size_t)i*49152,
-                upd_b2 + (size_t)i*3*F,
-                wbf_hi + oW1 + (size_t)(i+1)*16384, wbf_lo + oW1 + (size_t)(i+1)*16384,
-                msg_b1 + (size_t)(i+1)*F,
-                wbf_hi + oW2 + (size_t)(i+1)*49152, wbf_lo + oW2 + (size_t)(i+1)*49152,
-                msg_b2 + (size_t)(i+1)*3*F,
-                phi_buf,
-                nullptr, nullptr, nullptr, nullptr);
-        } else {
-            updphi_kernel<1><<<dim3(NP/32), dim3(256), 0, stream>>>(
-                s_buf, vout,
-                wbf_hi + oUV + (size_t)i*32768, wbf_lo + oUV + (size_t)i*32768,
-                wbf_hi + oU1 + (size_t)i*32768, wbf_lo + oU1 + (size_t)i*32768,
-                upd_b1 + (size_t)i*F,
-                wbf_hi + oU2 + (size_t)i*49152, wbf_lo + oU2 + (size_t)i*49152,
-                upd_b2 + (size_t)i*3*F,
-                wbf_hi + oRO, wbf_lo + oRO, robias,
-                nullptr, nullptr, nullptr,
-                nullptr,
-                ro_w2, ro_b2, molidx, out);
-        }
-        float* tmp = vin; vin = vout; vout = tmp;
-    }
+        phiA);
+
+    conv_kernel<1, 0><<<dim3(NP/32), dim3(256), 0, stream>>>(
+        s_buf, v0_buf, v1_buf,
+        phiA, edgerec, offsets,
+        rbf_w + (size_t)0*N_RBF*3*F, rbf_b + (size_t)0*3*F,
+        wbf_hi + oUV, wbf_lo + oUV,
+        wbf_hi + oU1, wbf_lo + oU1, upd_b1,
+        wbf_hi + oU2, wbf_lo + oU2, upd_b2,
+        wbf_hi + oW1 + 16384, wbf_lo + oW1 + 16384, msg_b1 + F,
+        wbf_hi + oW2 + 49152, wbf_lo + oW2 + 49152, msg_b2 + 3*F,
+        phiB,
+        nullptr, nullptr, nullptr, nullptr);
+
+    conv_kernel<0, 0><<<dim3(NP/32), dim3(256), 0, stream>>>(
+        s_buf, v1_buf, v0_buf,
+        phiB, edgerec, offsets,
+        rbf_w + (size_t)1*N_RBF*3*F, rbf_b + (size_t)1*3*F,
+        wbf_hi + oUV + 32768, wbf_lo + oUV + 32768,
+        wbf_hi + oU1 + 32768, wbf_lo + oU1 + 32768, upd_b1 + F,
+        wbf_hi + oU2 + 49152, wbf_lo + oU2 + 49152, upd_b2 + 3*F,
+        wbf_hi + oW1 + 2*16384, wbf_lo + oW1 + 2*16384, msg_b1 + 2*F,
+        wbf_hi + oW2 + 2*49152, wbf_lo + oW2 + 2*49152, msg_b2 + 2*3*F,
+        phiA,
+        nullptr, nullptr, nullptr, nullptr);
+
+    conv_kernel<0, 1><<<dim3(NP/32), dim3(256), 0, stream>>>(
+        s_buf, v0_buf, v1_buf,
+        phiA, edgerec, offsets,
+        rbf_w + (size_t)2*N_RBF*3*F, rbf_b + (size_t)2*3*F,
+        wbf_hi + oUV + 2*32768, wbf_lo + oUV + 2*32768,
+        wbf_hi + oU1 + 2*32768, wbf_lo + oU1 + 2*32768, upd_b1 + 2*F,
+        wbf_hi + oU2 + 2*49152, wbf_lo + oU2 + 2*49152, upd_b2 + 2*3*F,
+        wbf_hi + oRO, wbf_lo + oRO, robias,
+        nullptr, nullptr, nullptr,
+        nullptr,
+        ro_w2, ro_b2, molidx, out);
 }
```
